# Kernel tuning notes

Measured on AMD Instinct MI355X. Metric: run time of the kernel, lower is better.

Reference implementation:

```python
import jax, jax.numpy as jnp
import numpy as np
import math

B, N, H, C = 1, 2048, 8, 128
PQ, PV, R, CS, CZ = 8, 12, 2, 256, 128
CZ4 = CZ // 4
INF = 1e5
EPS = 1e-8
SOFTPLUS_INV_1 = 0.541324854612918


def _quat_to_rot(q):
    q = q / jnp.linalg.norm(q, axis=-1, keepdims=True)
    w, x, y, z = q[..., 0], q[..., 1], q[..., 2], q[..., 3]
    return jnp.stack([
        jnp.stack([1 - 2 * (y * y + z * z), 2 * (x * y - z * w), 2 * (x * z + y * w)], -1),
        jnp.stack([2 * (x * y + z * w), 1 - 2 * (x * x + z * z), 2 * (y * z - x * w)], -1),
        jnp.stack([2 * (x * z - y * w), 2 * (y * z + x * w), 1 - 2 * (x * x + y * y)], -1),
    ], -2)


def setup_inputs() -> dict:
    key = jax.random.key(0)
    ks = jax.random.split(key, 16)
    rn = lambda k, shape, s=1.0: jax.random.normal(k, shape, dtype=jnp.float32) * s
    hc = H * C
    return dict(
        s=rn(ks[0], (B, N, CS)),
        z_factor_1=rn(ks[1], (B, N, R, CZ)),
        z_factor_2=rn(ks[2], (B, N, R, CZ)),
        rot=_quat_to_rot(rn(ks[3], (B, N, 4))),
        trans=rn(ks[4], (B, N, 3)),
        mask=jnp.ones((B, N), dtype=bool),
        w_q=rn(ks[5], (hc, CS), 0.02), b_q=jnp.zeros((hc,), jnp.float32),
        w_kv=rn(ks[6], (2 * hc, CS), 0.02), b_kv=jnp.zeros((2 * hc,), jnp.float32),
        w_qp=rn(ks[7], (H * PQ * 3, CS), 0.02), b_qp=jnp.zeros((H * PQ * 3,), jnp.float32),
        w_kvp=rn(ks[8], (H * (PQ + PV) * 3, CS), 0.02), b_kvp=jnp.zeros((H * (PQ + PV) * 3,), jnp.float32),
        w_b=rn(ks[9], (H, CZ), 0.02), b_b=jnp.zeros((H,), jnp.float32),
        w_dz=rn(ks[10], (CZ4, CZ), 0.02), b_dz=jnp.zeros((CZ4,), jnp.float32),
        head_weights=jnp.full((H,), SOFTPLUS_INV_1, dtype=jnp.float32),
        w_out=rn(ks[11], (CS, H * (CZ4 + C + 4 * PV)), 0.02), b_out=jnp.zeros((CS,), jnp.float32),
    )


def _lin(x, w, b):
    return x @ w.T + b


def _ipa(s, z1, z2, rot, trans, mask, w_q, b_q, w_kv, b_kv, w_qp, b_qp,
         w_kvp, b_kvp, w_b, b_b, w_dz, b_dz, head_weights, w_out, b_out):
    q = _lin(s, w_q, b_q).reshape(B, N, H, C)
    kv = _lin(s, w_kv, b_kv).reshape(B, N, H, 2 * C)
    k, v = kv[..., :C], kv[..., C:]
    # local points -> global frame: x_glob = R x_loc + t
    qp = _lin(s, w_qp, b_qp).reshape(B, N, H * PQ, 3)
    qp = (jnp.einsum('bnij,bnpj->bnpi', rot, qp) + trans[:, :, None, :]).reshape(B, N, H, PQ, 3)
    kvp = _lin(s, w_kvp, b_kvp).reshape(B, N, H * (PQ + PV), 3)
    kvp = (jnp.einsum('bnij,bnpj->bnpi', rot, kvp) + trans[:, :, None, :]).reshape(B, N, H, PQ + PV, 3)
    kp, vp = kvp[..., :PQ, :], kvp[..., PQ:, :]
    # head weights: softplus init to 1, AF2 scaling sqrt(1/(3*(PQ*9/2)))
    hw = jax.nn.softplus(head_weights) * math.sqrt(1.0 / (3 * (PQ * 9.0 / 2)))
    # low-rank pair bias factors
    b1 = _lin(z1, w_b, b_b)   # [B,N,R,H]
    b2 = _lin(z2, w_b, b_b)
    z1d = _lin(z1, w_dz, b_dz)  # [B,N,R,CZ4]
    z2d = _lin(z2, w_dz, b_dz)
    # logits: scalar QK + point-distance + low-rank pair bias
    scalar = jnp.einsum('bihc,bjhc->bhij', q, k) * math.sqrt(1.0 / (3 * C))
    ptdot = jnp.einsum('bihpx,bjhpx->bhij', qp, kp)
    qn = jnp.sum(qp * qp, axis=(-1, -2))  # [B,N,H]
    kn = jnp.sum(kp * kp, axis=(-1, -2))
    pt_term = hw[None, :, None, None] * (
        ptdot - 0.5 * qn.transpose(0, 2, 1)[:, :, :, None] - 0.5 * kn.transpose(0, 2, 1)[:, :, None, :])
    pair = jnp.einsum('birh,bjrh->bhij', b1, b2)
    mask_bias = jnp.where(mask, 0.0, -INF)[:, None, None, :]
    a = jax.nn.softmax(scalar + pt_term + pair + mask_bias, axis=-1)  # [B,H,N,N]
    # outputs
    o = jnp.einsum('bhij,bjhc->bihc', a, v).reshape(B, N, H * C)
    opt = jnp.einsum('bhij,bjhpx->bihpx', a, vp)  # global-frame points
    opt_loc = jnp.einsum('bnji,bnhpj->bnhpi', rot, opt - trans[:, :, None, None, :])  # R^T (x - t)
    opt_norm = jnp.sqrt(jnp.sum(opt_loc * opt_loc, axis=-1) + EPS)  # [B,N,H,PV]
    oz = jnp.einsum('bhij,bjrc->bihrc', a, z2d)
    opair = jnp.sum(oz * z1d[:, :, None, :, :], axis=3)  # [B,N,H,CZ4]
    feats = jnp.concatenate([
        o,
        opt_loc[..., 0].reshape(B, N, H * PV),
        opt_loc[..., 1].reshape(B, N, H * PV),
        opt_loc[..., 2].reshape(B, N, H * PV),
        opt_norm.reshape(B, N, H * PV),
        opair.reshape(B, N, H * CZ4),
    ], axis=-1)
    return _lin(feats, w_out, b_out)  # [B,N,CS]


def reference(s, z_factor_1, z_factor_2, rot, trans, mask, w_q, b_q, w_kv, b_kv,
              w_qp, b_qp, w_kvp, b_kvp, w_b, b_b, w_dz, b_dz, head_weights,
              w_out, b_out):
    return _ipa(s, z_factor_1, z_factor_2, rot, trans, mask, w_q, b_q, w_kv, b_kv,
                w_qp, b_qp, w_kvp, b_kvp, w_b, b_b, w_dz, b_dz, head_weights,
                w_out, b_out)
```

## Files before the change

### kernel.cpp

```cpp
#include <hip/hip_runtime.h>
#include <math.h>

#define NN   2048
#define HH   8
#define CC   128
#define PQn  8
#define PVn  12
#define RRn  2
#define CSn  256
#define CZn  128
#define CZ4n 32
#define HC   (HH*CC)
#define FEAT (HC + 4*HH*PVn + HH*CZ4n)
#define DA   160
#define DVP  256
#define DVU  240
#define QKV  3840
#define LOG2E 1.4426950408889634f

typedef unsigned short ushort_t;
#define AS1 __attribute__((address_space(1)))
#define AS3 __attribute__((address_space(3)))

using bfrag = __attribute__((ext_vector_type(8))) short;
using ffrag = __attribute__((ext_vector_type(4))) float;

__device__ inline ushort_t f2bf(float x) {
    union { float f; unsigned int u; } v; v.f = x;
    unsigned int r = v.u + 0x7fffu + ((v.u >> 16) & 1u);
    return (ushort_t)(r >> 16);
}
__device__ inline float bf2f(ushort_t x) {
    union { unsigned int u; float f; } v; v.u = ((unsigned int)x) << 16; return v.f;
}

struct CvtArgs {
    const float4* src[12];
    ushort4* dst[12];
    int n4[12];
};
__global__ __launch_bounds__(256) void cvtn_kernel(CvtArgs a,
    float4* __restrict__ outp, const float4* __restrict__ bias4)
{
    int i = blockIdx.x * 256 + threadIdx.x;
    if (i < NN * CSn / 4) {
        outp[i] = bias4[i & 63];
        return;
    }
    i -= NN * CSn / 4;
#pragma unroll
    for (int k = 0; k < 12; ++k) {
        if (i < a.n4[k]) {
            ushort4 o;
            if (a.src[k]) {
                float4 v = a.src[k][i];
                o = make_ushort4(f2bf(v.x), f2bf(v.y), f2bf(v.z), f2bf(v.w));
            } else {
                o = make_ushort4(0, 0, 0, 0);
            }
            a.dst[k][i] = o;
            return;
        }
        i -= a.n4[k];
    }
}

__global__ __launch_bounds__(256) void bgemm_kernel(
    const ushort_t* __restrict__ A, size_t sA,
    const ushort_t* __restrict__ B, size_t sB,
    void* __restrict__ Cv, size_t sC,
    const float* __restrict__ bias, size_t sBias,
    int ldk, int kOff, int kOffPerZ, int kLen, int ldc, int obf, int atomicOut)
{
    const int z = blockIdx.z;
    A += (size_t)z * sA;
    B += (size_t)z * sB;
    const float* bp = bias ? (bias + (size_t)z * sBias) : nullptr;
    const int k0beg = kOff + z * kOffPerZ;
    const int r0 = blockIdx.y * 128;
    const int c0 = blockIdx.x * 128;
    __shared__ __align__(16) ushort_t lA[128 * 32];
    __shared__ __align__(16) ushort_t lB[128 * 32];
    const int tid = threadIdx.x;
    const int w = tid >> 6, lane = tid & 63;
    const int wm = (w >> 1) * 64, wn = (w & 1) * 64;
    const int lrA = lane >> 2;
    const int lcA = (lane & 3) * 8;
    ffrag acc[4][4] = {};

    for (int k0 = k0beg; k0 < k0beg + kLen; k0 += 32) {
#pragma unroll
        for (int t = 0; t < 2; ++t) {
            int instr = w * 2 + t;
            int r = instr * 16 + lrA;
            const ushort_t* ga = A + (size_t)(r0 + r) * ldk + k0 + lcA;
            const ushort_t* gb = B + (size_t)(c0 + r) * ldk + k0 + lcA;
            __builtin_amdgcn_global_load_lds((const AS1 void*)ga,
                (AS3 void*)((AS3 ushort_t*)&lA[instr * 512 + lane * 8]), 16, 0, 0);
            __builtin_amdgcn_global_load_lds((const AS1 void*)gb,
                (AS3 void*)((AS3 ushort_t*)&lB[instr * 512 + lane * 8]), 16, 0, 0);
        }
        __syncthreads();
        bfrag af[4], bf[4];
#pragma unroll
        for (int mi = 0; mi < 4; ++mi)
            af[mi] = *(const bfrag*)&lA[(wm + mi * 16 + (lane & 15)) * 32 + (lane >> 4) * 8];
#pragma unroll
        for (int ni = 0; ni < 4; ++ni)
            bf[ni] = *(const bfrag*)&lB[(wn + ni * 16 + (lane & 15)) * 32 + (lane >> 4) * 8];
#pragma unroll
        for (int mi = 0; mi < 4; ++mi)
#pragma unroll
            for (int ni = 0; ni < 4; ++ni)
                acc[mi][ni] = __builtin_amdgcn_mfma_f32_16x16x32_bf16(af[mi], bf[ni], acc[mi][ni], 0, 0, 0);
        __syncthreads();
    }
#pragma unroll
    for (int mi = 0; mi < 4; ++mi) {
#pragma unroll
        for (int ni = 0; ni < 4; ++ni) {
            int col = c0 + wn + ni * 16 + (lane & 15);
            float bv = bp ? bp[col] : 0.f;
#pragma unroll
            for (int rr = 0; rr < 4; ++rr) {
                int row = r0 + wm + mi * 16 + (lane >> 4) * 4 + rr;
                float val = acc[mi][ni][rr] + bv;
                if (atomicOut)
                    unsafeAtomicAdd(&((float*)Cv)[(size_t)z * sC + (size_t)row * ldc + col], val);
                else if (obf)
                    ((ushort_t*)Cv)[(size_t)z * sC + (size_t)row * ldc + col] = f2bf(val);
                else
                    ((float*)Cv)[(size_t)z * sC + (size_t)row * ldc + col] = val;
            }
        }
    }
}

__global__ __launch_bounds__(256) void mgemm_kernel(
    const ushort_t* __restrict__ A0, const ushort_t* __restrict__ B0,
    ushort_t* __restrict__ C0,
    const ushort_t* __restrict__ A1, const ushort_t* __restrict__ B1,
    ushort_t* __restrict__ C1)
{
    const int bx = blockIdx.x;
    const ushort_t *A, *B;
    ushort_t* C;
    int ldk, kLen, ldc, r0, c0;
    if (bx < 480) {
        A = A0; B = B0; C = C0;
        ldk = CSn; kLen = CSn; ldc = QKV;
        r0 = (bx / 30) * 128;
        c0 = (bx % 30) * 128;
    } else {
        int i = bx - 480;
        A = A1; B = B1; C = C1;
        ldk = CZn; kLen = CZn; ldc = 128;
        r0 = i * 128;
        c0 = 0;
    }
    __shared__ __align__(16) ushort_t lA[128 * 32];
    __shared__ __align__(16) ushort_t lB[128 * 32];
    const int tid = threadIdx.x;
    const int w = tid >> 6, lane = tid & 63;
    const int wm = (w >> 1) * 64, wn = (w & 1) * 64;
    const int lrA = lane >> 2;
    const int lcA = (lane & 3) * 8;
    ffrag acc[4][4] = {};

    for (int k0 = 0; k0 < kLen; k0 += 32) {
#pragma unroll
        for (int t = 0; t < 2; ++t) {
            int instr = w * 2 + t;
            int r = instr * 16 + lrA;
            const ushort_t* ga = A + (size_t)(r0 + r) * ldk + k0 + lcA;
            const ushort_t* gb = B + (size_t)(c0 + r) * ldk + k0 + lcA;
            __builtin_amdgcn_global_load_lds((const AS1 void*)ga,
                (AS3 void*)((AS3 ushort_t*)&lA[instr * 512 + lane * 8]), 16, 0, 0);
            __builtin_amdgcn_global_load_lds((const AS1 void*)gb,
                (AS3 void*)((AS3 ushort_t*)&lB[instr * 512 + lane * 8]), 16, 0, 0);
        }
        __syncthreads();
        bfrag af[4], bf[4];
#pragma unroll
        for (int mi = 0; mi < 4; ++mi)
            af[mi] = *(const bfrag*)&lA[(wm + mi * 16 + (lane & 15)) * 32 + (lane >> 4) * 8];
#pragma unroll
        for (int ni = 0; ni < 4; ++ni)
            bf[ni] = *(const bfrag*)&lB[(wn + ni * 16 + (lane & 15)) * 32 + (lane >> 4) * 8];
#pragma unroll
        for (int mi = 0; mi < 4; ++mi)
#pragma unroll
            for (int ni = 0; ni < 4; ++ni)
                acc[mi][ni] = __builtin_amdgcn_mfma_f32_16x16x32_bf16(af[mi], bf[ni], acc[mi][ni], 0, 0, 0);
        __syncthreads();
    }
#pragma unroll
    for (int mi = 0; mi < 4; ++mi) {
#pragma unroll
        for (int ni = 0; ni < 4; ++ni) {
            int col = c0 + wn + ni * 16 + (lane & 15);
#pragma unroll
            for (int rr = 0; rr < 4; ++rr) {
                int row = r0 + wm + mi * 16 + (lane >> 4) * 4 + rr;
                C[(size_t)row * ldc + col] = f2bf(acc[mi][ni][rr]);
            }
        }
    }
}

__global__ __launch_bounds__(256) void prep_kernel(
    const ushort_t* __restrict__ qkv,
    const ushort_t* __restrict__ zproj,
    const float* __restrict__ b_q, const float* __restrict__ b_kv,
    const float* __restrict__ b_qp, const float* __restrict__ b_kvp,
    const float* __restrict__ b_b, const float* __restrict__ b_dz,
    const float* __restrict__ rot, const float* __restrict__ trans,
    const float* __restrict__ hwts,
    ushort_t* __restrict__ qaug, ushort_t* __restrict__ kaug,
    ushort_t* __restrict__ vaug)
{
    const int i = blockIdx.x;
    const int tid = threadIdx.x;
    __shared__ float R[9], t[3];
    __shared__ float qp_l[192], kp_l[192], vp_l[288];
    __shared__ float kn_s[8], hw_s[8];
    __shared__ __align__(16) ushort_t qa_s[8 * DA];
    __shared__ __align__(16) ushort_t ka_s[8 * DA];
    __shared__ __align__(16) ushort_t va_s[8 * DVP];
    if (tid < 9) R[tid] = rot[i*9 + tid];
    if (tid < 3) t[tid] = trans[i*3 + tid];
    if (tid < 8) {
        hw_s[tid] = log1pf(expf(hwts[tid])) * 0.09622504486493763f;
        kn_s[tid] = 0.f;
    }
    __syncthreads();
    if (tid < 64) {
        const ushort_t* v = qkv + (size_t)i*QKV + 3072 + tid*3;
        float vx = bf2f(v[0]) + b_qp[tid*3+0];
        float vy = bf2f(v[1]) + b_qp[tid*3+1];
        float vz = bf2f(v[2]) + b_qp[tid*3+2];
        float X = R[0]*vx + R[1]*vy + R[2]*vz + t[0];
        float Y = R[3]*vx + R[4]*vy + R[5]*vz + t[1];
        float Z = R[6]*vx + R[7]*vy + R[8]*vz + t[2];
        qp_l[tid*3+0] = X; qp_l[tid*3+1] = Y; qp_l[tid*3+2] = Z;
    } else if (tid < 224) {
        int p = tid - 64;
        int h = p / 20, pp = p % 20;
        const ushort_t* v = qkv + (size_t)i*QKV + 3264 + p*3;
        float vx = bf2f(v[0]) + b_kvp[p*3+0];
        float vy = bf2f(v[1]) + b_kvp[p*3+1];
        float vz = bf2f(v[2]) + b_kvp[p*3+2];
        float X = R[0]*vx + R[1]*vy + R[2]*vz + t[0];
        float Y = R[3]*vx + R[4]*vy + R[5]*vz + t[1];
        float Z = R[6]*vx + R[7]*vy + R[8]*vz + t[2];
        if (pp < 8) {
            int b = (h*8 + pp) * 3;
            kp_l[b+0] = X; kp_l[b+1] = Y; kp_l[b+2] = Z;
            atomicAdd(&kn_s[h], X*X + Y*Y + Z*Z);
        } else {
            int b = (h*12 + pp - 8) * 3;
            vp_l[b+0] = X; vp_l[b+1] = Y; vp_l[b+2] = Z;
        }
    }
    __syncthreads();

    const float QS = 0.05103103630798288f * LOG2E;
    if (tid < 128) {
        int h = tid >> 4, d = (tid & 15) * 8;
        bfrag q8 = *(const bfrag*)(qkv + (size_t)i*QKV + h*128 + d);
        bfrag k8 = *(const bfrag*)(qkv + (size_t)i*QKV + 1024 + h*256 + d);
        ushort_t qo[8], ko[8];
#pragma unroll
        for (int e = 0; e < 8; ++e) {
            qo[e] = f2bf(QS * (bf2f((ushort_t)q8[e]) + b_q[h*128 + d + e]));
            ko[e] = f2bf(bf2f((ushort_t)k8[e]) + b_kv[h*256 + d + e]);
        }
        *(bfrag*)&qa_s[h*DA + d] = *(bfrag*)qo;
        *(bfrag*)&ka_s[h*DA + d] = *(bfrag*)ko;
    }
    {
        int h = tid >> 5, d = 128 + (tid & 31);
        float qv, kv2;
        if (d < 152) {
            qv  = hw_s[h] * LOG2E * qp_l[h*24 + d - 128];
            kv2 = kp_l[h*24 + d - 128];
        } else if (d < 154) {
            int r = d - 152;
            qv  = LOG2E * (bf2f(zproj[(size_t)(i*2 + r)*128 + h]) + b_b[h]);
            kv2 = bf2f(zproj[(size_t)(4096 + i*2 + r)*128 + h]) + b_b[h];
        } else if (d == 154) {
            qv  = LOG2E;
            kv2 = -0.5f * hw_s[h] * kn_s[h];
        } else { qv = 0.f; kv2 = 0.f; }
        qa_s[h*DA + d] = f2bf(qv);
        ka_s[h*DA + d] = f2bf(kv2);
    }
    if (tid < 128) {
        int h = tid >> 4, d = (tid & 15) * 8;
        bfrag v8 = *(const bfrag*)(qkv + (size_t)i*QKV + 1024 + h*256 + 128 + d);
        ushort_t vo[8];
#pragma unroll
        for (int e = 0; e < 8; ++e)
            vo[e] = f2bf(bf2f((ushort_t)v8[e]) + b_kv[h*256 + 128 + d + e]);
        *(bfrag*)&va_s[h*DVP + d] = *(bfrag*)vo;
    }
#pragma unroll
    for (int k = 0; k < 4; ++k) {
        int idx = k * 256 + tid;
        int h = idx >> 7, d = 128 + (idx & 127);
        float v;
        if (d < 164)       v = vp_l[h*36 + d - 128];
        else if (d < 196)  v = bf2f(zproj[(size_t)(4096 + i*2 + 0)*128 + 8 + d - 164]) + b_dz[d - 164];
        else if (d < 228)  v = bf2f(zproj[(size_t)(4096 + i*2 + 1)*128 + 8 + d - 196]) + b_dz[d - 196];
        else if (d == 239) v = 1.0f;
        else               v = 0.f;
        va_s[h*DVP + d] = f2bf(v);
    }
    __syncthreads();

    for (int idx = tid; idx < 576; idx += 256) {
        if (idx < 160) {
            int h = idx / 20, dg = (idx - h*20) * 8;
            *(bfrag*)(qaug + ((size_t)h*NN + i) * DA + dg) = *(const bfrag*)&qa_s[h*DA + dg];
        } else if (idx < 320) {
            int r = idx - 160;
            int h = r / 20, dg = (r - h*20) * 8;
            *(bfrag*)(kaug + ((size_t)h*NN + i) * DA + dg) = *(const bfrag*)&ka_s[h*DA + dg];
        } else {
            int r = idx - 320;
            int h = r >> 5, dg = (r & 31) * 8;
            *(bfrag*)(vaug + ((size_t)h*NN + i) * DVP + dg) = *(const bfrag*)&va_s[h*DVP + dg];
        }
    }
}

__global__ __launch_bounds__(256) void transpose_kernel(
    const ushort_t* __restrict__ in, ushort_t* __restrict__ out)
{
    const int z = blockIdx.z;
    in  += (size_t)z * NN * DVP;
    out += (size_t)z * NN * DVP;
    const int i0 = blockIdx.x * 64;
    const int d0 = blockIdx.y * 64;
    __shared__ __align__(8) ushort_t tb[64][72];
    const int tid = threadIdx.x;
#pragma unroll
    for (int p = 0; p < 4; ++p) {
        int idx = p * 256 + tid;
        int r = idx >> 4, sg = idx & 15;
        ushort4 v = *(const ushort4*)(in + (size_t)(i0 + r) * DVP + d0 + sg * 4);
        *(ushort4*)&tb[r][sg * 4] = v;
    }
    __syncthreads();
#pragma unroll
    for (int p = 0; p < 4; ++p) {
        int idx = p * 256 + tid;
        int d = idx >> 4, ig = idx & 15;
        ushort4 v = make_ushort4(tb[ig*4+0][d], tb[ig*4+1][d],
                                 tb[ig*4+2][d], tb[ig*4+3][d]);
        *(ushort4*)(out + (size_t)(d0 + d) * NN + i0 + ig * 4) = v;
    }
}

__global__ __launch_bounds__(1024, 4) void flash_kernel(
    const ushort_t* __restrict__ qaug,
    const ushort_t* __restrict__ kaug,
    const ushort_t* __restrict__ vaugT,
    ushort_t* __restrict__ Opart,
    float* __restrict__ Lpart)
{
    const int bid = blockIdx.x;
    const int G = bid & 15;
    const int m = bid >> 4;
    const int h = G >> 1;
    const int g = G & 1;
    const int i0 = m * 128;

    __shared__ __align__(16) ushort_t Kt[2][64 * 168];
    __shared__ __align__(16) ushort_t Vt[2][DVU * 72];
    __shared__ __align__(16) ushort_t Pl[2][128 * 72];

    const int tid = threadIdx.x;
    const int w = tid >> 6, lane = tid & 63;
    const int quad = lane >> 4, lc = lane & 15;
    const int rq = w >> 1, jq = w & 1;
    const int rh = w >> 2, dh = (w >> 1) & 1, jc = w & 1;

    const ushort_t* qh = qaug + (size_t)h * NN * DA;
    const ushort_t* kh = kaug + (size_t)h * NN * DA;
    const ushort_t* vh = vaugT + (size_t)h * DVP * NN;

    const int j0g = g * 1024;
    const int iK0 = tid, iK1 = 1024 + tid;
    const int rK0 = iK0 / 21, oK0 = iK0 - rK0 * 21;
    const int rK1 = iK1 / 21, oK1 = iK1 - rK1 * 21;
    const bool vK1 = (tid < 320);
    const ushort_t* kS0 = kh + (size_t)(j0g + rK0) * DA + (oK0 < 20 ? oK0 * 8 : 0);
    const ushort_t* kS1 = kh + (size_t)(j0g + rK1) * DA + (oK1 < 20 ? oK1 * 8 : 0);
    const int iV0 = tid, iV1 = 1024 + tid, iV2 = 2048 + tid;
    const int rV0 = iV0 / 9, oV0 = iV0 - rV0 * 9;
    const int rV1 = iV1 / 9, oV1 = iV1 - rV1 * 9;
    const int rV2 = iV2 / 9, oV2 = iV2 - rV2 * 9;
    const bool vV2 = (tid < 112);
    const ushort_t* vS0 = vh + (size_t)rV0 * NN + j0g + (oV0 < 8 ? oV0 * 8 : 0);
    const ushort_t* vS1 = vh + (size_t)rV1 * NN + j0g + (oV1 < 8 ? oV1 * 8 : 0);
    const ushort_t* vS2 = vh + (size_t)(vV2 ? rV2 : 0) * NN + j0g + (oV2 < 8 ? oV2 * 8 : 0);

    auto stageK = [&](ushort_t* dst) {
        __builtin_amdgcn_global_load_lds((const AS1 void*)kS0,
            (AS3 void*)((AS3 ushort_t*)&dst[iK0 * 8]), 16, 0, 0);
        if (vK1)
            __builtin_amdgcn_global_load_lds((const AS1 void*)kS1,
                (AS3 void*)((AS3 ushort_t*)&dst[iK1 * 8]), 16, 0, 0);
        kS0 += 64 * DA; kS1 += 64 * DA;
    };
    auto stageV = [&](ushort_t* dst) {
        __builtin_amdgcn_global_load_lds((const AS1 void*)vS0,
            (AS3 void*)((AS3 ushort_t*)&dst[iV0 * 8]), 16, 0, 0);
        __builtin_amdgcn_global_load_lds((const AS1 void*)vS1,
            (AS3 void*)((AS3 ushort_t*)&dst[iV1 * 8]), 16, 0, 0);
        if (vV2)
            __builtin_amdgcn_global_load_lds((const AS1 void*)vS2,
                (AS3 void*)((AS3 ushort_t*)&dst[iV2 * 8]), 16, 0, 0);
        vS0 += 64; vS1 += 64; vS2 += 64;
    };

    bfrag qf[5];
#pragma unroll
    for (int ks = 0; ks < 5; ++ks)
        qf[ks] = *(const bfrag*)(qh + (size_t)(i0 + rq * 16 + lc) * DA + ks * 32 + quad * 8);

    ffrag acc[2][8];
#pragma unroll
    for (int mi = 0; mi < 2; ++mi)
#pragma unroll
        for (int t = 0; t < 8; ++t)
            acc[mi][t] = (ffrag){0.f, 0.f, 0.f, 0.f};

    stageK(Kt[0]);
    stageV(Vt[0]);
    __syncthreads();

    for (int it = 0; it < 16; ++it) {
        const int cur = it & 1;

        if (it < 15) stageK(Kt[cur ^ 1]);

        ffrag sf[2];
        sf[0] = (ffrag){0.f, 0.f, 0.f, 0.f};
        sf[1] = (ffrag){0.f, 0.f, 0.f, 0.f};
        const ushort_t* ktb = &Kt[cur][(jq * 32 + lc) * 168 + quad * 8];
        __builtin_amdgcn_s_setprio(1);
#pragma unroll
        for (int ks = 0; ks < 5; ++ks) {
            bfrag kf0 = *(const bfrag*)(ktb + ks * 32);
            bfrag kf1 = *(const bfrag*)(ktb + 16 * 168 + ks * 32);
            sf[0] = __builtin_amdgcn_mfma_f32_16x16x32_bf16(qf[ks], kf0, sf[0], 0, 0, 0);
            sf[1] = __builtin_amdgcn_mfma_f32_16x16x32_bf16(qf[ks], kf1, sf[1], 0, 0, 0);
        }

        if (it > 0) {
            const ushort_t* Plp = Pl[cur ^ 1];
            bfrag pf0 = *(const bfrag*)&Plp[(rh * 32 + lc) * 72 + jc * 32 + quad * 8];
            bfrag pf1 = *(const bfrag*)&Plp[(rh * 32 + 16 + lc) * 72 + jc * 32 + quad * 8];
            const ushort_t* vtb = &Vt[cur ^ 1][(dh * 128 + lc) * 72 + jc * 32 + quad * 8];
#pragma unroll
            for (int t = 0; t < 8; ++t) {
                if (dh && t == 7) continue;
                bfrag vf = *(const bfrag*)(vtb + t * 16 * 72);
                acc[0][t] = __builtin_amdgcn_mfma_f32_16x16x32_bf16(pf0, vf, acc[0][t], 0, 0, 0);
                acc[1][t] = __builtin_amdgcn_mfma_f32_16x16x32_bf16(pf1, vf, acc[1][t], 0, 0, 0);
            }
        }
        __builtin_amdgcn_s_setprio(0);

        {
            ushort_t* Plc = Pl[cur];
#pragma unroll
            for (int jt = 0; jt < 2; ++jt)
#pragma unroll
                for (int rr = 0; rr < 4; ++rr)
                    Plc[(rq * 16 + quad * 4 + rr) * 72 + jq * 32 + jt * 16 + lc] =
                        f2bf(exp2f(sf[jt][rr]));
        }

        __syncthreads();

        if (it < 15) stageV(Vt[cur ^ 1]);
    }

    {
        const ushort_t* Plp = Pl[1];
        bfrag pf0 = *(const bfrag*)&Plp[(rh * 32 + lc) * 72 + jc * 32 + quad * 8];
        bfrag pf1 = *(const bfrag*)&Plp[(rh * 32 + 16 + lc) * 72 + jc * 32 + quad * 8];
        const ushort_t* vtb = &Vt[1][(dh * 128 + lc) * 72 + jc * 32 + quad * 8];
#pragma unroll
        for (int t = 0; t < 8; ++t) {
            if (dh && t == 7) continue;
            bfrag vf = *(const bfrag*)(vtb + t * 16 * 72);
            acc[0][t] = __builtin_amdgcn_mfma_f32_16x16x32_bf16(pf0, vf, acc[0][t], 0, 0, 0);
            acc[1][t] = __builtin_amdgcn_mfma_f32_16x16x32_bf16(pf1, vf, acc[1][t], 0, 0, 0);
        }
    }

    ushort_t* scratch = (ushort_t*)Vt;
    const int pw = w >> 1;
    __syncthreads();
    if (jc == 1) {
        ushort_t tmp[64];
#pragma unroll
        for (int mi = 0; mi < 2; ++mi)
#pragma unroll
            for (int t = 0; t < 8; ++t)
#pragma unroll
                for (int rr = 0; rr < 4; ++rr)
                    tmp[mi*32 + t*4 + rr] = f2bf(acc[mi][t][rr]);
#pragma unroll
        for (int j = 0; j < 8; ++j)
            *(bfrag*)&scratch[pw * 4096 + j * 512 + lane * 8] = *(bfrag*)&tmp[j * 8];
    }
    __syncthreads();
    if (jc == 0) {
#pragma unroll
        for (int j = 0; j < 8; ++j) {
            bfrag v = *(const bfrag*)&scratch[pw * 4096 + j * 512 + lane * 8];
#pragma unroll
            for (int e = 0; e < 8; ++e) {
                int idx = j * 8 + e;
                acc[idx >> 5][(idx >> 2) & 7][idx & 3] += bf2f((ushort_t)v[e]);
            }
        }
        ushort_t* Ob = Opart + ((size_t)g * HH + h) * NN * DVU;
#pragma unroll
        for (int mi = 0; mi < 2; ++mi)
#pragma unroll
            for (int t = 0; t < 8; ++t) {
                if (dh && t == 7) continue;
                int dt = dh * 8 + t;
#pragma unroll
                for (int rr = 0; rr < 4; ++rr) {
                    int row = i0 + rh * 32 + mi * 16 + quad * 4 + rr;
                    Ob[(size_t)row * DVU + dt * 16 + lc] = f2bf(acc[mi][t][rr]);
                }
            }
        size_t sb = ((size_t)g * HH + h) * NN;
        if (dh == 1 && lc == 15) {
#pragma unroll
            for (int mi = 0; mi < 2; ++mi)
#pragma unroll
                for (int rr = 0; rr < 4; ++rr)
                    Lpart[sb + i0 + rh * 32 + mi * 16 + quad * 4 + rr] = acc[mi][6][rr];
        }
    }
}

__global__ __launch_bounds__(256) void combine_kernel(
    const ushort_t* __restrict__ Opart, const float* __restrict__ Lpart,
    const ushort_t* __restrict__ zproj, const float* __restrict__ b_dz,
    const float* __restrict__ rot, const float* __restrict__ trans,
    ushort_t* __restrict__ feats)
{
    const int i = blockIdx.x;
    const int tid = threadIdx.x;
    __shared__ float wgt8[8];
    __shared__ float Ol[8][DVU];
    if (tid < 8) {
        float l0 = Lpart[(size_t)(0 * HH + tid) * NN + i];
        float l1 = Lpart[(size_t)(1 * HH + tid) * NN + i];
        wgt8[tid] = 1.f / (l0 + l1);
    }
    __syncthreads();
    {
        int h = tid >> 5;
        int dg0 = tid & 31;
        for (int dg = dg0; dg < 60; dg += 32) {
            int d = dg * 4;
            ushort4 u0 = *(const ushort4*)&Opart[(((size_t)0 * HH + h) * NN + i) * DVU + d];
            ushort4 u1 = *(const ushort4*)&Opart[(((size_t)1 * HH + h) * NN + i) * DVU + d];
            float wv = wgt8[h];
            Ol[h][d+0] = (bf2f(u0.x) + bf2f(u1.x)) * wv;
            Ol[h][d+1] = (bf2f(u0.y) + bf2f(u1.y)) * wv;
            Ol[h][d+2] = (bf2f(u0.z) + bf2f(u1.z)) * wv;
            Ol[h][d+3] = (bf2f(u0.w) + bf2f(u1.w)) * wv;
        }
    }
    __syncthreads();

    ushort_t* f = feats + (size_t)i * FEAT;
    {
        int h = tid >> 5;
        int c = (tid * 4) & 127;
        ushort4 o4 = make_ushort4(f2bf(Ol[h][c]), f2bf(Ol[h][c+1]),
                                  f2bf(Ol[h][c+2]), f2bf(Ol[h][c+3]));
        *(ushort4*)(f + tid * 4) = o4;
    }
    if (tid < 96) {
        int h = tid / 12, p = tid % 12;
        const float* Rm = rot + i * 9;
        float ox = Ol[h][128 + p*3 + 0] - trans[i*3 + 0];
        float oy = Ol[h][128 + p*3 + 1] - trans[i*3 + 1];
        float oz = Ol[h][128 + p*3 + 2] - trans[i*3 + 2];
        float lx = Rm[0]*ox + Rm[3]*oy + Rm[6]*oz;
        float ly = Rm[1]*ox + Rm[4]*oy + Rm[7]*oz;
        float lz = Rm[2]*ox + Rm[5]*oy + Rm[8]*oz;
        float nrm = sqrtf(lx*lx + ly*ly + lz*lz + 1e-8f);
        f[1024 + 0*96 + tid] = f2bf(lx);
        f[1024 + 1*96 + tid] = f2bf(ly);
        f[1024 + 2*96 + tid] = f2bf(lz);
        f[1024 + 3*96 + tid] = f2bf(nrm);
    }
    {
        int h = tid >> 5, c = tid & 31;
        float z1d0 = bf2f(zproj[(size_t)(i*2 + 0)*128 + 8 + c]) + b_dz[c];
        float z1d1 = bf2f(zproj[(size_t)(i*2 + 1)*128 + 8 + c]) + b_dz[c];
        f[1408 + tid] = f2bf(Ol[h][164 + c] * z1d0 + Ol[h][196 + c] * z1d1);
    }
}

extern "C" void kernel_launch(void* const* d_in, const int* in_sizes, int n_in,
                              void* d_out, int out_size, void* d_ws, size_t ws_size,
                              hipStream_t stream) {
    const float* s     = (const float*)d_in[0];
    const float* z1    = (const float*)d_in[1];
    const float* z2    = (const float*)d_in[2];
    const float* rot   = (const float*)d_in[3];
    const float* trans = (const float*)d_in[4];
    const float* w_q   = (const float*)d_in[6];
    const float* b_q   = (const float*)d_in[7];
    const float* w_kv  = (const float*)d_in[8];
    const float* b_kv  = (const float*)d_in[9];
    const float* w_qp  = (const float*)d_in[10];
    const float* b_qp  = (const float*)d_in[11];
    const float* w_kvp = (const float*)d_in[12];
    const float* b_kvp = (const float*)d_in[13];
    const float* w_b   = (const float*)d_in[14];
    const float* b_b   = (const float*)d_in[15];
    const float* w_dz  = (const float*)d_in[16];
    const float* b_dz  = (const float*)d_in[17];
    const float* hwts  = (const float*)d_in[18];
    const float* w_out = (const float*)d_in[19];
    const float* b_out = (const float*)d_in[20];
    float* out = (float*)d_out;

    char* base = (char*)d_ws;
    const size_t OPART_BYTES = (size_t)4*HH*NN*DVU*2;
    char* S = base;
    ushort_t* s_bf  = (ushort_t*)(S);
    ushort_t* z_bf  = (ushort_t*)(S + 1048576);
    ushort_t* wall  = (ushort_t*)(S + 1048576 + 2097152);
    ushort_t* wz    = (ushort_t*)(S + 1048576 + 2097152 + 1966080);
    ushort_t* qkv   = (ushort_t*)(S + 1048576 + 2097152 + 1966080 + 32768);
    ushort_t* vaug  = (ushort_t*)(S + 1048576 + 2097152 + 1966080 + 32768 + 15728640);
    ushort_t* Opart = (ushort_t*)(S);
    char* P = base + OPART_BYTES;
    size_t off = 0;
    auto alloc = [&](size_t bytes) -> void* {
        void* p = P + off;
        off += (bytes + 255) & ~(size_t)255;
        return p;
    };
    ushort_t* wout_bf = (ushort_t*)alloc((size_t)CSn*FEAT*2);
    ushort_t* zproj   = (ushort_t*)alloc((size_t)8192*128*2);
    ushort_t* qaug    = (ushort_t*)alloc((size_t)HH*NN*DA*2);
    ushort_t* kaug    = (ushort_t*)alloc((size_t)HH*NN*DA*2);
    ushort_t* vaugT   = (ushort_t*)alloc((size_t)HH*NN*DVP*2);
    float*    Mpart   = (float*)alloc((size_t)4*HH*NN*4);
    float*    Lpart   = (float*)alloc((size_t)4*HH*NN*4);
    ushort_t* feats   = (ushort_t*)alloc((size_t)NN*FEAT*2);
    (void)Mpart;

    CvtArgs ca;
    int j = 0; int tot = 0;
    auto job = [&](const float* src, ushort_t* dst, int nElem) {
        ca.src[j] = (const float4*)src; ca.dst[j] = (ushort4*)dst; ca.n4[j] = nElem/4;
        tot += nElem/4; ++j;
    };
    job(s,     s_bf,              NN*CSn);
    job(z1,    z_bf,              4096*128);
    job(z2,    z_bf + 4096*128,   4096*128);
    job(w_q,   wall,              1024*256);
    job(w_kv,  wall + 1024*256,   2048*256);
    job(w_qp,  wall + 3072*256,   192*256);
    job(w_kvp, wall + 3264*256,   480*256);
    job(w_out, wout_bf,           CSn*FEAT);
    job(nullptr, wall + 3744*256, 96*256);
    job(w_b,   wz,                8*128);
    job(w_dz,  wz + 8*128,        32*128);
    job(nullptr, wz + 40*128,     88*128);
    tot += NN*CSn/4;
    cvtn_kernel<<<(tot + 255)/256, 256, 0, stream>>>(ca, (float4*)out, (const float4*)b_out);

    mgemm_kernel<<<544, 256, 0, stream>>>(s_bf, wall, qkv, z_bf, wz, zproj);

    prep_kernel<<<NN, 256, 0, stream>>>(qkv, zproj,
                                        b_q, b_kv, b_qp, b_kvp, b_b, b_dz,
                                        rot, trans, hwts, qaug, kaug, vaug);
    transpose_kernel<<<dim3(NN/64, DVP/64, HH), 256, 0, stream>>>(vaug, vaugT);

    flash_kernel<<<256, 1024, 0, stream>>>(
        qaug, kaug, vaugT, Opart, Lpart);

    combine_kernel<<<NN, 256, 0, stream>>>(Opart, Lpart, zproj, b_dz,
                                           rot, trans, feats);

    bgemm_kernel<<<dim3(CSn/128, NN/128, 4), 256, 0, stream>>>(
        feats, 0, wout_bf, 0, out, 0, nullptr, 0,
        FEAT, 0, FEAT/4, FEAT/4, CSn, 0, 1);
}
```

Before: 194.0 us.

## Fuse all stages into one persistent megakernel with grid-wide atomic barriers

Replaces the seven separate launches (convert, projection GEMMs, prep, transpose, flash attention, combine, output GEMM) with a single persistent kernel of 256 blocks of 1024 threads. The stages are separated by a software grid barrier built on an atomic counter. Each stage's work is remapped onto four 256-thread crews per block. This removes launch overhead and the inter-kernel gaps, but depends on all 256 blocks being co-resident. It also forces every stage onto the same block shape and shared-memory budget, which may lower per-stage efficiency.

```diff
diff --git a/kernel.cpp b/kernel.cpp
--- a/kernel.cpp
+++ b/kernel.cpp
@@ -34,436 +34,400 @@
     union { unsigned int u; float f; } v; v.u = ((unsigned int)x) << 16; return v.f;
 }
 
+#define GLOAD(src, dst) __builtin_amdgcn_global_load_lds((const AS1 void*)(src), \
+    (AS3 void*)((AS3 ushort_t*)(dst)), 16, 0, 0)
+
 struct CvtArgs {
     const float4* src[12];
     ushort4* dst[12];
     int n4[12];
 };
-__global__ __launch_bounds__(256) void cvtn_kernel(CvtArgs a,
-    float4* __restrict__ outp, const float4* __restrict__ bias4)
-{
-    int i = blockIdx.x * 256 + threadIdx.x;
-    if (i < NN * CSn / 4) {
-        outp[i] = bias4[i & 63];
-        return;
-    }
-    i -= NN * CSn / 4;
-#pragma unroll
-    for (int k = 0; k < 12; ++k) {
-        if (i < a.n4[k]) {
-            ushort4 o;
-            if (a.src[k]) {
-                float4 v = a.src[k][i];
-                o = make_ushort4(f2bf(v.x), f2bf(v.y), f2bf(v.z), f2bf(v.w));
-            } else {
-                o = make_ushort4(0, 0, 0, 0);
-            }
-            a.dst[k][i] = o;
-            return;
-        }
-        i -= a.n4[k];
-    }
+
+__device__ inline void gsync(unsigned* cnt, unsigned target) {
+    __syncthreads();
+    if (threadIdx.x == 0) {
+        __threadfence();
+        atomicAdd(cnt, 1u);
+        while (atomicAdd(cnt, 0u) < target) __builtin_amdgcn_s_sleep(8);
+        __threadfence();
+    }
+    __syncthreads();
 }
 
-__global__ __launch_bounds__(256) void bgemm_kernel(
-    const ushort_t* __restrict__ A, size_t sA,
-    const ushort_t* __restrict__ B, size_t sB,
-    void* __restrict__ Cv, size_t sC,
-    const float* __restrict__ bias, size_t sBias,
-    int ldk, int kOff, int kOffPerZ, int kLen, int ldc, int obf, int atomicOut)
-{
-    const int z = blockIdx.z;
-    A += (size_t)z * sA;
-    B += (size_t)z * sB;
-    const float* bp = bias ? (bias + (size_t)z * sBias) : nullptr;
-    const int k0beg = kOff + z * kOffPerZ;
-    const int r0 = blockIdx.y * 128;
-    const int c0 = blockIdx.x * 128;
-    __shared__ __align__(16) ushort_t lA[128 * 32];
-    __shared__ __align__(16) ushort_t lB[128 * 32];
-    const int tid = threadIdx.x;
-    const int w = tid >> 6, lane = tid & 63;
-    const int wm = (w >> 1) * 64, wn = (w & 1) * 64;
-    const int lrA = lane >> 2;
-    const int lcA = (lane & 3) * 8;
-    ffrag acc[4][4] = {};
-
-    for (int k0 = k0beg; k0 < k0beg + kLen; k0 += 32) {
-#pragma unroll
-        for (int t = 0; t < 2; ++t) {
-            int instr = w * 2 + t;
-            int r = instr * 16 + lrA;
-            const ushort_t* ga = A + (size_t)(r0 + r) * ldk + k0 + lcA;
-            const ushort_t* gb = B + (size_t)(c0 + r) * ldk + k0 + lcA;
-            __builtin_amdgcn_global_load_lds((const AS1 void*)ga,
-                (AS3 void*)((AS3 ushort_t*)&lA[instr * 512 + lane * 8]), 16, 0, 0);
-            __builtin_amdgcn_global_load_lds((const AS1 void*)gb,
-                (AS3 void*)((AS3 ushort_t*)&lB[instr * 512 + lane * 8]), 16, 0, 0);
-        }
-        __syncthreads();
-        bfrag af[4], bf[4];
-#pragma unroll
-        for (int mi = 0; mi < 4; ++mi)
-            af[mi] = *(const bfrag*)&lA[(wm + mi * 16 + (lane & 15)) * 32 + (lane >> 4) * 8];
-#pragma unroll
-        for (int ni = 0; ni < 4; ++ni)
-            bf[ni] = *(const bfrag*)&lB[(wn + ni * 16 + (lane & 15)) * 32 + (lane >> 4) * 8];
-#pragma unroll
-        for (int mi = 0; mi < 4; ++mi)
-#pragma unroll
-            for (int ni = 0; ni < 4; ++ni)
-                acc[mi][ni] = __builtin_amdgcn_mfma_f32_16x16x32_bf16(af[mi], bf[ni], acc[mi][ni], 0, 0, 0);
-        __syncthreads();
-    }
-#pragma unroll
-    for (int mi = 0; mi < 4; ++mi) {
-#pragma unroll
-        for (int ni = 0; ni < 4; ++ni) {
-            int col = c0 + wn + ni * 16 + (lane & 15);
-            float bv = bp ? bp[col] : 0.f;
-#pragma unroll
-            for (int rr = 0; rr < 4; ++rr) {
-                int row = r0 + wm + mi * 16 + (lane >> 4) * 4 + rr;
-                float val = acc[mi][ni][rr] + bv;
-                if (atomicOut)
-                    unsafeAtomicAdd(&((float*)Cv)[(size_t)z * sC + (size_t)row * ldc + col], val);
-                else if (obf)
-                    ((ushort_t*)Cv)[(size_t)z * sC + (size_t)row * ldc + col] = f2bf(val);
-                else
-                    ((float*)Cv)[(size_t)z * sC + (size_t)row * ldc + col] = val;
-            }
-        }
-    }
-}
-
-__global__ __launch_bounds__(256) void mgemm_kernel(
-    const ushort_t* __restrict__ A0, const ushort_t* __restrict__ B0,
-    ushort_t* __restrict__ C0,
-    const ushort_t* __restrict__ A1, const ushort_t* __restrict__ B1,
-    ushort_t* __restrict__ C1)
-{
-    const int bx = blockIdx.x;
-    const ushort_t *A, *B;
-    ushort_t* C;
-    int ldk, kLen, ldc, r0, c0;
-    if (bx < 480) {
-        A = A0; B = B0; C = C0;
-        ldk = CSn; kLen = CSn; ldc = QKV;
-        r0 = (bx / 30) * 128;
-        c0 = (bx % 30) * 128;
-    } else {
-        int i = bx - 480;
-        A = A1; B = B1; C = C1;
-        ldk = CZn; kLen = CZn; ldc = 128;
-        r0 = i * 128;
-        c0 = 0;
-    }
-    __shared__ __align__(16) ushort_t lA[128 * 32];
-    __shared__ __align__(16) ushort_t lB[128 * 32];
-    const int tid = threadIdx.x;
-    const int w = tid >> 6, lane = tid & 63;
-    const int wm = (w >> 1) * 64, wn = (w & 1) * 64;
-    const int lrA = lane >> 2;
-    const int lcA = (lane & 3) * 8;
-    ffrag acc[4][4] = {};
-
-    for (int k0 = 0; k0 < kLen; k0 += 32) {
-#pragma unroll
-        for (int t = 0; t < 2; ++t) {
-            int instr = w * 2 + t;
-            int r = instr * 16 + lrA;
-            const ushort_t* ga = A + (size_t)(r0 + r) * ldk + k0 + lcA;
-            const ushort_t* gb = B + (size_t)(c0 + r) * ldk + k0 + lcA;
-            __builtin_amdgcn_global_load_lds((const AS1 void*)ga,
-                (AS3 void*)((AS3 ushort_t*)&lA[instr * 512 + lane * 8]), 16, 0, 0);
-            __builtin_amdgcn_global_load_lds((const AS1 void*)gb,
-                (AS3 void*)((AS3 ushort_t*)&lB[instr * 512 + lane * 8]), 16, 0, 0);
-        }
-        __syncthreads();
-        bfrag af[4], bf[4];
-#pragma unroll
-        for (int mi = 0; mi < 4; ++mi)
-            af[mi] = *(const bfrag*)&lA[(wm + mi * 16 + (lane & 15)) * 32 + (lane >> 4) * 8];
-#pragma unroll
-        for (int ni = 0; ni < 4; ++ni)
-            bf[ni] = *(const bfrag*)&lB[(wn + ni * 16 + (lane & 15)) * 32 + (lane >> 4) * 8];
-#pragma unroll
-        for (int mi = 0; mi < 4; ++mi)
-#pragma unroll
-            for (int ni = 0; ni < 4; ++ni)
-                acc[mi][ni] = __builtin_amdgcn_mfma_f32_16x16x32_bf16(af[mi], bf[ni], acc[mi][ni], 0, 0, 0);
-        __syncthreads();
-    }
-#pragma unroll
-    for (int mi = 0; mi < 4; ++mi) {
-#pragma unroll
-        for (int ni = 0; ni < 4; ++ni) {
-            int col = c0 + wn + ni * 16 + (lane & 15);
-#pragma unroll
-            for (int rr = 0; rr < 4; ++rr) {
-                int row = r0 + wm + mi * 16 + (lane >> 4) * 4 + rr;
-                C[(size_t)row * ldc + col] = f2bf(acc[mi][ni][rr]);
-            }
-        }
-    }
-}
-
-__global__ __launch_bounds__(256) void prep_kernel(
-    const ushort_t* __restrict__ qkv,
-    const ushort_t* __restrict__ zproj,
+struct PrepShm {
+    float R[9], t[3];
+    float qp_l[192], kp_l[192], vp_l[288];
+    float kn_s[8], hw_s[8];
+    __align__(16) ushort_t qa_s[8 * DA];
+    __align__(16) ushort_t ka_s[8 * DA];
+    __align__(16) ushort_t va_s[8 * DVP];
+};
+struct CombShm {
+    float wgt8[8];
+    float Ol[8][DVU];
+};
+
+__global__ __launch_bounds__(1024, 4) void mega_kernel(
+    CvtArgs ca, float4* __restrict__ outp, const float4* __restrict__ bias4, int cvtTot,
+    const ushort_t* __restrict__ s_bf, const ushort_t* __restrict__ wall,
+    ushort_t* __restrict__ qkv, const ushort_t* __restrict__ z_bf,
+    const ushort_t* __restrict__ wz, ushort_t* __restrict__ zproj,
     const float* __restrict__ b_q, const float* __restrict__ b_kv,
     const float* __restrict__ b_qp, const float* __restrict__ b_kvp,
     const float* __restrict__ b_b, const float* __restrict__ b_dz,
     const float* __restrict__ rot, const float* __restrict__ trans,
     const float* __restrict__ hwts,
     ushort_t* __restrict__ qaug, ushort_t* __restrict__ kaug,
-    ushort_t* __restrict__ vaug)
+    ushort_t* __restrict__ vaug, ushort_t* __restrict__ vaugT,
+    ushort_t* __restrict__ Opart, float* __restrict__ Lpart,
+    ushort_t* __restrict__ feats, const ushort_t* __restrict__ wout_bf,
+    float* __restrict__ out, unsigned* __restrict__ syncnt)
 {
-    const int i = blockIdx.x;
+    __shared__ __align__(16) char smem[148992];
     const int tid = threadIdx.x;
-    __shared__ float R[9], t[3];
-    __shared__ float qp_l[192], kp_l[192], vp_l[288];
-    __shared__ float kn_s[8], hw_s[8];
-    __shared__ __align__(16) ushort_t qa_s[8 * DA];
-    __shared__ __align__(16) ushort_t ka_s[8 * DA];
-    __shared__ __align__(16) ushort_t va_s[8 * DVP];
-    if (tid < 9) R[tid] = rot[i*9 + tid];
-    if (tid < 3) t[tid] = trans[i*3 + tid];
-    if (tid < 8) {
-        hw_s[tid] = log1pf(expf(hwts[tid])) * 0.09622504486493763f;
-        kn_s[tid] = 0.f;
-    }
-    __syncthreads();
-    if (tid < 64) {
-        const ushort_t* v = qkv + (size_t)i*QKV + 3072 + tid*3;
-        float vx = bf2f(v[0]) + b_qp[tid*3+0];
-        float vy = bf2f(v[1]) + b_qp[tid*3+1];
-        float vz = bf2f(v[2]) + b_qp[tid*3+2];
-        float X = R[0]*vx + R[1]*vy + R[2]*vz + t[0];
-        float Y = R[3]*vx + R[4]*vy + R[5]*vz + t[1];
-        float Z = R[6]*vx + R[7]*vy + R[8]*vz + t[2];
-        qp_l[tid*3+0] = X; qp_l[tid*3+1] = Y; qp_l[tid*3+2] = Z;
-    } else if (tid < 224) {
-        int p = tid - 64;
-        int h = p / 20, pp = p % 20;
-        const ushort_t* v = qkv + (size_t)i*QKV + 3264 + p*3;
-        float vx = bf2f(v[0]) + b_kvp[p*3+0];
-        float vy = bf2f(v[1]) + b_kvp[p*3+1];
-        float vz = bf2f(v[2]) + b_kvp[p*3+2];
-        float X = R[0]*vx + R[1]*vy + R[2]*vz + t[0];
-        float Y = R[3]*vx + R[4]*vy + R[5]*vz + t[1];
-        float Z = R[6]*vx + R[7]*vy + R[8]*vz + t[2];
-        if (pp < 8) {
-            int b = (h*8 + pp) * 3;
-            kp_l[b+0] = X; kp_l[b+1] = Y; kp_l[b+2] = Z;
-            atomicAdd(&kn_s[h], X*X + Y*Y + Z*Z);
-        } else {
-            int b = (h*12 + pp - 8) * 3;
-            vp_l[b+0] = X; vp_l[b+1] = Y; vp_l[b+2] = Z;
-        }
-    }
-    __syncthreads();
-
-    const float QS = 0.05103103630798288f * LOG2E;
-    if (tid < 128) {
-        int h = tid >> 4, d = (tid & 15) * 8;
-        bfrag q8 = *(const bfrag*)(qkv + (size_t)i*QKV + h*128 + d);
-        bfrag k8 = *(const bfrag*)(qkv + (size_t)i*QKV + 1024 + h*256 + d);
-        ushort_t qo[8], ko[8];
-#pragma unroll
-        for (int e = 0; e < 8; ++e) {
-            qo[e] = f2bf(QS * (bf2f((ushort_t)q8[e]) + b_q[h*128 + d + e]));
-            ko[e] = f2bf(bf2f((ushort_t)k8[e]) + b_kv[h*256 + d + e]);
-        }
-        *(bfrag*)&qa_s[h*DA + d] = *(bfrag*)qo;
-        *(bfrag*)&ka_s[h*DA + d] = *(bfrag*)ko;
-    }
+    const int bid = blockIdx.x;
+    const int crew = tid >> 8, ctid = tid & 255;
+
     {
-        int h = tid >> 5, d = 128 + (tid & 31);
-        float qv, kv2;
-        if (d < 152) {
-            qv  = hw_s[h] * LOG2E * qp_l[h*24 + d - 128];
-            kv2 = kp_l[h*24 + d - 128];
-        } else if (d < 154) {
-            int r = d - 152;
-            qv  = LOG2E * (bf2f(zproj[(size_t)(i*2 + r)*128 + h]) + b_b[h]);
-            kv2 = bf2f(zproj[(size_t)(4096 + i*2 + r)*128 + h]) + b_b[h];
-        } else if (d == 154) {
-            qv  = LOG2E;
-            kv2 = -0.5f * hw_s[h] * kn_s[h];
-        } else { qv = 0.f; kv2 = 0.f; }
-        qa_s[h*DA + d] = f2bf(qv);
-        ka_s[h*DA + d] = f2bf(kv2);
-    }
-    if (tid < 128) {
-        int h = tid >> 4, d = (tid & 15) * 8;
-        bfrag v8 = *(const bfrag*)(qkv + (size_t)i*QKV + 1024 + h*256 + 128 + d);
-        ushort_t vo[8];
-#pragma unroll
-        for (int e = 0; e < 8; ++e)
-            vo[e] = f2bf(bf2f((ushort_t)v8[e]) + b_kv[h*256 + 128 + d + e]);
-        *(bfrag*)&va_s[h*DVP + d] = *(bfrag*)vo;
-    }
-#pragma unroll
-    for (int k = 0; k < 4; ++k) {
-        int idx = k * 256 + tid;
-        int h = idx >> 7, d = 128 + (idx & 127);
-        float v;
-        if (d < 164)       v = vp_l[h*36 + d - 128];
-        else if (d < 196)  v = bf2f(zproj[(size_t)(4096 + i*2 + 0)*128 + 8 + d - 164]) + b_dz[d - 164];
-        else if (d < 228)  v = bf2f(zproj[(size_t)(4096 + i*2 + 1)*128 + 8 + d - 196]) + b_dz[d - 196];
-        else if (d == 239) v = 1.0f;
-        else               v = 0.f;
-        va_s[h*DVP + d] = f2bf(v);
-    }
-    __syncthreads();
-
-    for (int idx = tid; idx < 576; idx += 256) {
-        if (idx < 160) {
-            int h = idx / 20, dg = (idx - h*20) * 8;
-            *(bfrag*)(qaug + ((size_t)h*NN + i) * DA + dg) = *(const bfrag*)&qa_s[h*DA + dg];
-        } else if (idx < 320) {
-            int r = idx - 160;
-            int h = r / 20, dg = (r - h*20) * 8;
-            *(bfrag*)(kaug + ((size_t)h*NN + i) * DA + dg) = *(const bfrag*)&ka_s[h*DA + dg];
-        } else {
-            int r = idx - 320;
-            int h = r >> 5, dg = (r & 31) * 8;
-            *(bfrag*)(vaug + ((size_t)h*NN + i) * DVP + dg) = *(const bfrag*)&va_s[h*DVP + dg];
-        }
-    }
-}
-
-__global__ __launch_bounds__(256) void transpose_kernel(
-    const ushort_t* __restrict__ in, ushort_t* __restrict__ out)
-{
-    const int z = blockIdx.z;
-    in  += (size_t)z * NN * DVP;
-    out += (size_t)z * NN * DVP;
-    const int i0 = blockIdx.x * 64;
-    const int d0 = blockIdx.y * 64;
-    __shared__ __align__(8) ushort_t tb[64][72];
-    const int tid = threadIdx.x;
-#pragma unroll
-    for (int p = 0; p < 4; ++p) {
-        int idx = p * 256 + tid;
-        int r = idx >> 4, sg = idx & 15;
-        ushort4 v = *(const ushort4*)(in + (size_t)(i0 + r) * DVP + d0 + sg * 4);
-        *(ushort4*)&tb[r][sg * 4] = v;
-    }
-    __syncthreads();
-#pragma unroll
-    for (int p = 0; p < 4; ++p) {
-        int idx = p * 256 + tid;
-        int d = idx >> 4, ig = idx & 15;
-        ushort4 v = make_ushort4(tb[ig*4+0][d], tb[ig*4+1][d],
-                                 tb[ig*4+2][d], tb[ig*4+3][d]);
-        *(ushort4*)(out + (size_t)(d0 + d) * NN + i0 + ig * 4) = v;
-    }
-}
-
-__global__ __launch_bounds__(1024, 4) void flash_kernel(
-    const ushort_t* __restrict__ qaug,
-    const ushort_t* __restrict__ kaug,
-    const ushort_t* __restrict__ vaugT,
-    ushort_t* __restrict__ Opart,
-    float* __restrict__ Lpart)
-{
-    const int bid = blockIdx.x;
-    const int G = bid & 15;
-    const int m = bid >> 4;
-    const int h = G >> 1;
-    const int g = G & 1;
-    const int i0 = m * 128;
-
-    __shared__ __align__(16) ushort_t Kt[2][64 * 168];
-    __shared__ __align__(16) ushort_t Vt[2][DVU * 72];
-    __shared__ __align__(16) ushort_t Pl[2][128 * 72];
-
-    const int tid = threadIdx.x;
-    const int w = tid >> 6, lane = tid & 63;
-    const int quad = lane >> 4, lc = lane & 15;
-    const int rq = w >> 1, jq = w & 1;
-    const int rh = w >> 2, dh = (w >> 1) & 1, jc = w & 1;
-
-    const ushort_t* qh = qaug + (size_t)h * NN * DA;
-    const ushort_t* kh = kaug + (size_t)h * NN * DA;
-    const ushort_t* vh = vaugT + (size_t)h * DVP * NN;
-
-    const int j0g = g * 1024;
-    const int iK0 = tid, iK1 = 1024 + tid;
-    const int rK0 = iK0 / 21, oK0 = iK0 - rK0 * 21;
-    const int rK1 = iK1 / 21, oK1 = iK1 - rK1 * 21;
-    const bool vK1 = (tid < 320);
-    const ushort_t* kS0 = kh + (size_t)(j0g + rK0) * DA + (oK0 < 20 ? oK0 * 8 : 0);
-    const ushort_t* kS1 = kh + (size_t)(j0g + rK1) * DA + (oK1 < 20 ? oK1 * 8 : 0);
-    const int iV0 = tid, iV1 = 1024 + tid, iV2 = 2048 + tid;
-    const int rV0 = iV0 / 9, oV0 = iV0 - rV0 * 9;
-    const int rV1 = iV1 / 9, oV1 = iV1 - rV1 * 9;
-    const int rV2 = iV2 / 9, oV2 = iV2 - rV2 * 9;
-    const bool vV2 = (tid < 112);
-    const ushort_t* vS0 = vh + (size_t)rV0 * NN + j0g + (oV0 < 8 ? oV0 * 8 : 0);
-    const ushort_t* vS1 = vh + (size_t)rV1 * NN + j0g + (oV1 < 8 ? oV1 * 8 : 0);
-    const ushort_t* vS2 = vh + (size_t)(vV2 ? rV2 : 0) * NN + j0g + (oV2 < 8 ? oV2 * 8 : 0);
-
-    auto stageK = [&](ushort_t* dst) {
-        __builtin_amdgcn_global_load_lds((const AS1 void*)kS0,
-            (AS3 void*)((AS3 ushort_t*)&dst[iK0 * 8]), 16, 0, 0);
-        if (vK1)
-            __builtin_amdgcn_global_load_lds((const AS1 void*)kS1,
-                (AS3 void*)((AS3 ushort_t*)&dst[iK1 * 8]), 16, 0, 0);
-        kS0 += 64 * DA; kS1 += 64 * DA;
-    };
-    auto stageV = [&](ushort_t* dst) {
-        __builtin_amdgcn_global_load_lds((const AS1 void*)vS0,
-            (AS3 void*)((AS3 ushort_t*)&dst[iV0 * 8]), 16, 0, 0);
-        __builtin_amdgcn_global_load_lds((const AS1 void*)vS1,
-            (AS3 void*)((AS3 ushort_t*)&dst[iV1 * 8]), 16, 0, 0);
-        if (vV2)
-            __builtin_amdgcn_global_load_lds((const AS1 void*)vS2,
-                (AS3 void*)((AS3 ushort_t*)&dst[iV2 * 8]), 16, 0, 0);
-        vS0 += 64; vS1 += 64; vS2 += 64;
-    };
-
-    bfrag qf[5];
-#pragma unroll
-    for (int ks = 0; ks < 5; ++ks)
-        qf[ks] = *(const bfrag*)(qh + (size_t)(i0 + rq * 16 + lc) * DA + ks * 32 + quad * 8);
-
-    ffrag acc[2][8];
-#pragma unroll
-    for (int mi = 0; mi < 2; ++mi)
-#pragma unroll
-        for (int t = 0; t < 8; ++t)
-            acc[mi][t] = (ffrag){0.f, 0.f, 0.f, 0.f};
-
-    stageK(Kt[0]);
-    stageV(Vt[0]);
-    __syncthreads();
-
-    for (int it = 0; it < 16; ++it) {
-        const int cur = it & 1;
-
-        if (it < 15) stageK(Kt[cur ^ 1]);
-
-        ffrag sf[2];
-        sf[0] = (ffrag){0.f, 0.f, 0.f, 0.f};
-        sf[1] = (ffrag){0.f, 0.f, 0.f, 0.f};
-        const ushort_t* ktb = &Kt[cur][(jq * 32 + lc) * 168 + quad * 8];
-        __builtin_amdgcn_s_setprio(1);
-#pragma unroll
-        for (int ks = 0; ks < 5; ++ks) {
-            bfrag kf0 = *(const bfrag*)(ktb + ks * 32);
-            bfrag kf1 = *(const bfrag*)(ktb + 16 * 168 + ks * 32);
-            sf[0] = __builtin_amdgcn_mfma_f32_16x16x32_bf16(qf[ks], kf0, sf[0], 0, 0, 0);
-            sf[1] = __builtin_amdgcn_mfma_f32_16x16x32_bf16(qf[ks], kf1, sf[1], 0, 0, 0);
-        }
-
-        if (it > 0) {
-            const ushort_t* Plp = Pl[cur ^ 1];
+        const int STRIDE = 256 * 1024;
+        for (int it = bid * 1024 + tid; it < cvtTot; it += STRIDE) {
+            int r = it;
+            if (r < NN * CSn / 4) { outp[r] = bias4[r & 63]; continue; }
+            r -= NN * CSn / 4;
+#pragma unroll
+            for (int k = 0; k < 12; ++k) {
+                if (r < ca.n4[k]) {
+                    ushort4 o;
+                    if (ca.src[k]) {
+                        float4 v = ca.src[k][r];
+                        o = make_ushort4(f2bf(v.x), f2bf(v.y), f2bf(v.z), f2bf(v.w));
+                    } else {
+                        o = make_ushort4(0, 0, 0, 0);
+                    }
+                    ca.dst[k][r] = o;
+                    r = -1; break;
+                }
+                r -= ca.n4[k];
+            }
+        }
+    }
+    gsync(syncnt, 256 * 1);
+
+    {
+        const int vb = bid + 256 * crew;
+        const bool active = vb < 544;
+        const ushort_t *A = s_bf, *B = wall;
+        ushort_t* C = qkv;
+        int ldk = CSn, kIters = 8, ldc = QKV, r0 = 0, c0 = 0;
+        if (vb < 480) { r0 = (vb / 30) * 128; c0 = (vb % 30) * 128; }
+        else if (active) { int i2 = vb - 480; A = z_bf; B = wz; C = zproj;
+                           ldk = CZn; kIters = 4; ldc = 128; r0 = i2 * 128; c0 = 0; }
+        ushort_t* lA = (ushort_t*)(smem + crew * 16384);
+        ushort_t* lB = lA + 4096;
+        const int w4 = ctid >> 6, lane = ctid & 63;
+        const int wm = (w4 >> 1) * 64, wn = (w4 & 1) * 64;
+        const int lrA = lane >> 2, lcA = (lane & 3) * 8;
+        ffrag acc[4][4] = {};
+        for (int kk = 0; kk < 8; ++kk) {
+            bool act = active && (kk < kIters);
+            if (act) {
+                int k0 = kk * 32;
+#pragma unroll
+                for (int t = 0; t < 2; ++t) {
+                    int instr = w4 * 2 + t;
+                    int r = instr * 16 + lrA;
+                    GLOAD(A + (size_t)(r0 + r) * ldk + k0 + lcA, &lA[instr * 512 + lane * 8]);
+                    GLOAD(B + (size_t)(c0 + r) * ldk + k0 + lcA, &lB[instr * 512 + lane * 8]);
+                }
+            }
+            __syncthreads();
+            if (act) {
+                bfrag af[4], bf[4];
+#pragma unroll
+                for (int mi = 0; mi < 4; ++mi)
+                    af[mi] = *(const bfrag*)&lA[(wm + mi * 16 + (lane & 15)) * 32 + (lane >> 4) * 8];
+#pragma unroll
+                for (int ni = 0; ni < 4; ++ni)
+                    bf[ni] = *(const bfrag*)&lB[(wn + ni * 16 + (lane & 15)) * 32 + (lane >> 4) * 8];
+#pragma unroll
+                for (int mi = 0; mi < 4; ++mi)
+#pragma unroll
+                    for (int ni = 0; ni < 4; ++ni)
+                        acc[mi][ni] = __builtin_amdgcn_mfma_f32_16x16x32_bf16(af[mi], bf[ni], acc[mi][ni], 0, 0, 0);
+            }
+            __syncthreads();
+        }
+        if (active) {
+#pragma unroll
+            for (int mi = 0; mi < 4; ++mi)
+#pragma unroll
+                for (int ni = 0; ni < 4; ++ni) {
+                    int col = c0 + wn + ni * 16 + (lane & 15);
+#pragma unroll
+                    for (int rr = 0; rr < 4; ++rr) {
+                        int row = r0 + wm + mi * 16 + (lane >> 4) * 4 + rr;
+                        C[(size_t)row * ldc + col] = f2bf(acc[mi][ni][rr]);
+                    }
+                }
+        }
+    }
+    gsync(syncnt, 256 * 2);
+
+    {
+        PrepShm* ps = (PrepShm*)(smem + crew * 12016);
+        for (int rep = 0; rep < 2; ++rep) {
+            const int i = bid * 8 + crew * 2 + rep;
+            if (ctid < 9) ps->R[ctid] = rot[i * 9 + ctid];
+            if (ctid < 3) ps->t[ctid] = trans[i * 3 + ctid];
+            if (ctid < 8) {
+                ps->hw_s[ctid] = log1pf(expf(hwts[ctid])) * 0.09622504486493763f;
+                ps->kn_s[ctid] = 0.f;
+            }
+            __syncthreads();
+            if (ctid < 64) {
+                const ushort_t* v = qkv + (size_t)i * QKV + 3072 + ctid * 3;
+                float vx = bf2f(v[0]) + b_qp[ctid * 3 + 0];
+                float vy = bf2f(v[1]) + b_qp[ctid * 3 + 1];
+                float vz = bf2f(v[2]) + b_qp[ctid * 3 + 2];
+                float X = ps->R[0] * vx + ps->R[1] * vy + ps->R[2] * vz + ps->t[0];
+                float Y = ps->R[3] * vx + ps->R[4] * vy + ps->R[5] * vz + ps->t[1];
+                float Z = ps->R[6] * vx + ps->R[7] * vy + ps->R[8] * vz + ps->t[2];
+                ps->qp_l[ctid * 3 + 0] = X; ps->qp_l[ctid * 3 + 1] = Y; ps->qp_l[ctid * 3 + 2] = Z;
+            } else if (ctid < 224) {
+                int p = ctid - 64;
+                int h = p / 20, pp = p % 20;
+                const ushort_t* v = qkv + (size_t)i * QKV + 3264 + p * 3;
+                float vx = bf2f(v[0]) + b_kvp[p * 3 + 0];
+                float vy = bf2f(v[1]) + b_kvp[p * 3 + 1];
+                float vz = bf2f(v[2]) + b_kvp[p * 3 + 2];
+                float X = ps->R[0] * vx + ps->R[1] * vy + ps->R[2] * vz + ps->t[0];
+                float Y = ps->R[3] * vx + ps->R[4] * vy + ps->R[5] * vz + ps->t[1];
+                float Z = ps->R[6] * vx + ps->R[7] * vy + ps->R[8] * vz + ps->t[2];
+                if (pp < 8) {
+                    int b = (h * 8 + pp) * 3;
+                    ps->kp_l[b + 0] = X; ps->kp_l[b + 1] = Y; ps->kp_l[b + 2] = Z;
+                    atomicAdd(&ps->kn_s[h], X * X + Y * Y + Z * Z);
+                } else {
+                    int b = (h * 12 + pp - 8) * 3;
+                    ps->vp_l[b + 0] = X; ps->vp_l[b + 1] = Y; ps->vp_l[b + 2] = Z;
+                }
+            }
+            __syncthreads();
+
+            const float QS = 0.05103103630798288f * LOG2E;
+            if (ctid < 128) {
+                int h = ctid >> 4, d = (ctid & 15) * 8;
+                bfrag q8 = *(const bfrag*)(qkv + (size_t)i * QKV + h * 128 + d);
+                bfrag k8 = *(const bfrag*)(qkv + (size_t)i * QKV + 1024 + h * 256 + d);
+                ushort_t qo[8], ko[8];
+#pragma unroll
+                for (int e = 0; e < 8; ++e) {
+                    qo[e] = f2bf(QS * (bf2f((ushort_t)q8[e]) + b_q[h * 128 + d + e]));
+                    ko[e] = f2bf(bf2f((ushort_t)k8[e]) + b_kv[h * 256 + d + e]);
+                }
+                *(bfrag*)&ps->qa_s[h * DA + d] = *(bfrag*)qo;
+                *(bfrag*)&ps->ka_s[h * DA + d] = *(bfrag*)ko;
+            }
+            {
+                int h = ctid >> 5, d = 128 + (ctid & 31);
+                float qv, kv2;
+                if (d < 152) {
+                    qv  = ps->hw_s[h] * LOG2E * ps->qp_l[h * 24 + d - 128];
+                    kv2 = ps->kp_l[h * 24 + d - 128];
+                } else if (d < 154) {
+                    int r = d - 152;
+                    qv  = LOG2E * (bf2f(zproj[(size_t)(i * 2 + r) * 128 + h]) + b_b[h]);
+                    kv2 = bf2f(zproj[(size_t)(4096 + i * 2 + r) * 128 + h]) + b_b[h];
+                } else if (d == 154) {
+                    qv  = LOG2E;
+                    kv2 = -0.5f * ps->hw_s[h] * ps->kn_s[h];
+                } else { qv = 0.f; kv2 = 0.f; }
+                ps->qa_s[h * DA + d] = f2bf(qv);
+                ps->ka_s[h * DA + d] = f2bf(kv2);
+            }
+            if (ctid < 128) {
+                int h = ctid >> 4, d = (ctid & 15) * 8;
+                bfrag v8 = *(const bfrag*)(qkv + (size_t)i * QKV + 1024 + h * 256 + 128 + d);
+                ushort_t vo[8];
+#pragma unroll
+                for (int e = 0; e < 8; ++e)
+                    vo[e] = f2bf(bf2f((ushort_t)v8[e]) + b_kv[h * 256 + 128 + d + e]);
+                *(bfrag*)&ps->va_s[h * DVP + d] = *(bfrag*)vo;
+            }
+#pragma unroll
+            for (int k = 0; k < 4; ++k) {
+                int idx = k * 256 + ctid;
+                int h = idx >> 7, d = 128 + (idx & 127);
+                float v;
+                if (d < 164)       v = ps->vp_l[h * 36 + d - 128];
+                else if (d < 196)  v = bf2f(zproj[(size_t)(4096 + i * 2 + 0) * 128 + 8 + d - 164]) + b_dz[d - 164];
+                else if (d < 228)  v = bf2f(zproj[(size_t)(4096 + i * 2 + 1) * 128 + 8 + d - 196]) + b_dz[d - 196];
+                else if (d == 239) v = 1.0f;
+                else               v = 0.f;
+                ps->va_s[h * DVP + d] = f2bf(v);
+            }
+            __syncthreads();
+
+            for (int idx = ctid; idx < 576; idx += 256) {
+                if (idx < 160) {
+                    int h = idx / 20, dg = (idx - h * 20) * 8;
+                    *(bfrag*)(qaug + ((size_t)h * NN + i) * DA + dg) = *(const bfrag*)&ps->qa_s[h * DA + dg];
+                } else if (idx < 320) {
+                    int r = idx - 160;
+                    int h = r / 20, dg = (r - h * 20) * 8;
+                    *(bfrag*)(kaug + ((size_t)h * NN + i) * DA + dg) = *(const bfrag*)&ps->ka_s[h * DA + dg];
+                } else {
+                    int r = idx - 320;
+                    int h = r >> 5, dg = (r & 31) * 8;
+                    *(bfrag*)(vaug + ((size_t)h * NN + i) * DVP + dg) = *(const bfrag*)&ps->va_s[h * DVP + dg];
+                }
+            }
+            __syncthreads();
+        }
+    }
+    gsync(syncnt, 256 * 3);
+
+    {
+        const int vb = bid + 256 * crew;
+        const int x = vb & 31, y = (vb >> 5) & 3, z = vb >> 7;
+        const ushort_t* in  = vaug  + (size_t)z * NN * DVP;
+        ushort_t*       outT = vaugT + (size_t)z * NN * DVP;
+        const int i0 = x * 64, d0 = y * 64;
+        ushort_t* tb = (ushort_t*)(smem + crew * 9216);
+#pragma unroll
+        for (int p = 0; p < 4; ++p) {
+            int idx = p * 256 + ctid;
+            int r = idx >> 4, sg = idx & 15;
+            ushort4 v = *(const ushort4*)(in + (size_t)(i0 + r) * DVP + d0 + sg * 4);
+            *(ushort4*)&tb[r * 72 + sg * 4] = v;
+        }
+        __syncthreads();
+#pragma unroll
+        for (int p = 0; p < 4; ++p) {
+            int idx = p * 256 + ctid;
+            int d = idx >> 4, ig = idx & 15;
+            ushort4 v = make_ushort4(tb[(ig * 4 + 0) * 72 + d], tb[(ig * 4 + 1) * 72 + d],
+                                     tb[(ig * 4 + 2) * 72 + d], tb[(ig * 4 + 3) * 72 + d]);
+            *(ushort4*)(outT + (size_t)(d0 + d) * NN + i0 + ig * 4) = v;
+        }
+    }
+    gsync(syncnt, 256 * 4);
+
+    {
+        ushort_t* const KtB = (ushort_t*)smem;
+        ushort_t* const VtB = (ushort_t*)smem + 21504;
+        ushort_t* const PlB = (ushort_t*)smem + 56064;
+#define KT(b)  (KtB + (b) * 10752)
+#define VT(b)  (VtB + (b) * 17280)
+#define PLBUF(b) (PlB + (b) * 9216)
+
+        const int G = bid & 15;
+        const int m = bid >> 4;
+        const int h = G >> 1;
+        const int g = G & 1;
+        const int i0 = m * 128;
+
+        const int w = tid >> 6, lane = tid & 63;
+        const int quad = lane >> 4, lc = lane & 15;
+        const int rq = w >> 1, jq = w & 1;
+        const int rh = w >> 2, dh = (w >> 1) & 1, jc = w & 1;
+
+        const ushort_t* qh = qaug + (size_t)h * NN * DA;
+        const ushort_t* kh = kaug + (size_t)h * NN * DA;
+        const ushort_t* vh = vaugT + (size_t)h * DVP * NN;
+
+        const int j0g = g * 1024;
+        const int iK0 = tid, iK1 = 1024 + tid;
+        const int rK0 = iK0 / 21, oK0 = iK0 - rK0 * 21;
+        const int rK1 = iK1 / 21, oK1 = iK1 - rK1 * 21;
+        const bool vK1 = (tid < 320);
+        const ushort_t* kS0 = kh + (size_t)(j0g + rK0) * DA + (oK0 < 20 ? oK0 * 8 : 0);
+        const ushort_t* kS1 = kh + (size_t)(j0g + rK1) * DA + (oK1 < 20 ? oK1 * 8 : 0);
+        const int iV0 = tid, iV1 = 1024 + tid, iV2 = 2048 + tid;
+        const int rV0 = iV0 / 9, oV0 = iV0 - rV0 * 9;
+        const int rV1 = iV1 / 9, oV1 = iV1 - rV1 * 9;
+        const int rV2 = iV2 / 9, oV2 = iV2 - rV2 * 9;
+        const bool vV2 = (tid < 112);
+        const ushort_t* vS0 = vh + (size_t)rV0 * NN + j0g + (oV0 < 8 ? oV0 * 8 : 0);
+        const ushort_t* vS1 = vh + (size_t)rV1 * NN + j0g + (oV1 < 8 ? oV1 * 8 : 0);
+        const ushort_t* vS2 = vh + (size_t)(vV2 ? rV2 : 0) * NN + j0g + (oV2 < 8 ? oV2 * 8 : 0);
+
+        auto stageK = [&](ushort_t* dst) {
+            GLOAD(kS0, &dst[iK0 * 8]);
+            if (vK1) GLOAD(kS1, &dst[iK1 * 8]);
+            kS0 += 64 * DA; kS1 += 64 * DA;
+        };
+        auto stageV = [&](ushort_t* dst) {
+            GLOAD(vS0, &dst[iV0 * 8]);
+            GLOAD(vS1, &dst[iV1 * 8]);
+            if (vV2) GLOAD(vS2, &dst[iV2 * 8]);
+            vS0 += 64; vS1 += 64; vS2 += 64;
+        };
+
+        bfrag qf[5];
+#pragma unroll
+        for (int ks = 0; ks < 5; ++ks)
+            qf[ks] = *(const bfrag*)(qh + (size_t)(i0 + rq * 16 + lc) * DA + ks * 32 + quad * 8);
+
+        ffrag acc[2][8];
+#pragma unroll
+        for (int mi = 0; mi < 2; ++mi)
+#pragma unroll
+            for (int t = 0; t < 8; ++t)
+                acc[mi][t] = (ffrag){0.f, 0.f, 0.f, 0.f};
+
+        stageK(KT(0));
+        stageV(VT(0));
+        __syncthreads();
+
+        for (int it = 0; it < 16; ++it) {
+            const int cur = it & 1;
+            if (it < 15) stageK(KT(cur ^ 1));
+
+            ffrag sf[2];
+            sf[0] = (ffrag){0.f, 0.f, 0.f, 0.f};
+            sf[1] = (ffrag){0.f, 0.f, 0.f, 0.f};
+            const ushort_t* ktb = KT(cur) + (jq * 32 + lc) * 168 + quad * 8;
+            __builtin_amdgcn_s_setprio(1);
+#pragma unroll
+            for (int ks = 0; ks < 5; ++ks) {
+                bfrag kf0 = *(const bfrag*)(ktb + ks * 32);
+                bfrag kf1 = *(const bfrag*)(ktb + 16 * 168 + ks * 32);
+                sf[0] = __builtin_amdgcn_mfma_f32_16x16x32_bf16(qf[ks], kf0, sf[0], 0, 0, 0);
+                sf[1] = __builtin_amdgcn_mfma_f32_16x16x32_bf16(qf[ks], kf1, sf[1], 0, 0, 0);
+            }
+            if (it > 0) {
+                const ushort_t* Plp = PLBUF(cur ^ 1);
+                bfrag pf0 = *(const bfrag*)&Plp[(rh * 32 + lc) * 72 + jc * 32 + quad * 8];
+                bfrag pf1 = *(const bfrag*)&Plp[(rh * 32 + 16 + lc) * 72 + jc * 32 + quad * 8];
+                const ushort_t* vtb = VT(cur ^ 1) + (dh * 128 + lc) * 72 + jc * 32 + quad * 8;
+#pragma unroll
+                for (int t = 0; t < 8; ++t) {
+                    if (dh && t == 7) continue;
+                    bfrag vf = *(const bfrag*)(vtb + t * 16 * 72);
+                    acc[0][t] = __builtin_amdgcn_mfma_f32_16x16x32_bf16(pf0, vf, acc[0][t], 0, 0, 0);
+                    acc[1][t] = __builtin_amdgcn_mfma_f32_16x16x32_bf16(pf1, vf, acc[1][t], 0, 0, 0);
+                }
+            }
+            __builtin_amdgcn_s_setprio(0);
+            {
+                ushort_t* Plc = PLBUF(cur);
+#pragma unroll
+                for (int jt = 0; jt < 2; ++jt)
+#pragma unroll
+                    for (int rr = 0; rr < 4; ++rr)
+                        Plc[(rq * 16 + quad * 4 + rr) * 72 + jq * 32 + jt * 16 + lc] =
+                            f2bf(exp2f(sf[jt][rr]));
+            }
+            __syncthreads();
+            if (it < 15) stageV(VT(cur ^ 1));
+        }
+
+        {
+            const ushort_t* Plp = PLBUF(1);
             bfrag pf0 = *(const bfrag*)&Plp[(rh * 32 + lc) * 72 + jc * 32 + quad * 8];
             bfrag pf1 = *(const bfrag*)&Plp[(rh * 32 + 16 + lc) * 72 + jc * 32 + quad * 8];
-            const ushort_t* vtb = &Vt[cur ^ 1][(dh * 128 + lc) * 72 + jc * 32 + quad * 8];
+            const ushort_t* vtb = VT(1) + (dh * 128 + lc) * 72 + jc * 32 + quad * 8;
 #pragma unroll
             for (int t = 0; t < 8; ++t) {
                 if (dh && t == 7) continue;
@@ -472,148 +436,177 @@
                 acc[1][t] = __builtin_amdgcn_mfma_f32_16x16x32_bf16(pf1, vf, acc[1][t], 0, 0, 0);
             }
         }
-        __builtin_amdgcn_s_setprio(0);
-
-        {
-            ushort_t* Plc = Pl[cur];
-#pragma unroll
-            for (int jt = 0; jt < 2; ++jt)
-#pragma unroll
-                for (int rr = 0; rr < 4; ++rr)
-                    Plc[(rq * 16 + quad * 4 + rr) * 72 + jq * 32 + jt * 16 + lc] =
-                        f2bf(exp2f(sf[jt][rr]));
-        }
-
+
+        ushort_t* scratch = VT(0);
+        const int pw = w >> 1;
         __syncthreads();
-
-        if (it < 15) stageV(Vt[cur ^ 1]);
-    }
+        if (jc == 1) {
+            ushort_t tmp[64];
+#pragma unroll
+            for (int mi = 0; mi < 2; ++mi)
+#pragma unroll
+                for (int t = 0; t < 8; ++t)
+#pragma unroll
+                    for (int rr = 0; rr < 4; ++rr)
+                        tmp[mi * 32 + t * 4 + rr] = f2bf(acc[mi][t][rr]);
+#pragma unroll
+            for (int j = 0; j < 8; ++j)
+                *(bfrag*)&scratch[pw * 4096 + j * 512 + lane * 8] = *(bfrag*)&tmp[j * 8];
+        }
+        __syncthreads();
+        if (jc == 0) {
+#pragma unroll
+            for (int j = 0; j < 8; ++j) {
+                bfrag v = *(const bfrag*)&scratch[pw * 4096 + j * 512 + lane * 8];
+#pragma unroll
+                for (int e = 0; e < 8; ++e) {
+                    int idx = j * 8 + e;
+                    acc[idx >> 5][(idx >> 2) & 7][idx & 3] += bf2f((ushort_t)v[e]);
+                }
+            }
+            ushort_t* Ob = Opart + ((size_t)g * HH + h) * NN * DVU;
+#pragma unroll
+            for (int mi = 0; mi < 2; ++mi)
+#pragma unroll
+                for (int t = 0; t < 8; ++t) {
+                    if (dh && t == 7) continue;
+                    int dt = dh * 8 + t;
+#pragma unroll
+                    for (int rr = 0; rr < 4; ++rr) {
+                        int row = i0 + rh * 32 + mi * 16 + quad * 4 + rr;
+                        Ob[(size_t)row * DVU + dt * 16 + lc] = f2bf(acc[mi][t][rr]);
+                    }
+                }
+            size_t sb = ((size_t)g * HH + h) * NN;
+            if (dh == 1 && lc == 15) {
+#pragma unroll
+                for (int mi = 0; mi < 2; ++mi)
+#pragma unroll
+                    for (int rr = 0; rr < 4; ++rr)
+                        Lpart[sb + i0 + rh * 32 + mi * 16 + quad * 4 + rr] = acc[mi][6][rr];
+            }
+        }
+#undef KT
+#undef VT
+#undef PLBUF
+    }
+    gsync(syncnt, 256 * 5);
 
     {
-        const ushort_t* Plp = Pl[1];
-        bfrag pf0 = *(const bfrag*)&Plp[(rh * 32 + lc) * 72 + jc * 32 + quad * 8];
-        bfrag pf1 = *(const bfrag*)&Plp[(rh * 32 + 16 + lc) * 72 + jc * 32 + quad * 8];
-        const ushort_t* vtb = &Vt[1][(dh * 128 + lc) * 72 + jc * 32 + quad * 8];
-#pragma unroll
-        for (int t = 0; t < 8; ++t) {
-            if (dh && t == 7) continue;
-            bfrag vf = *(const bfrag*)(vtb + t * 16 * 72);
-            acc[0][t] = __builtin_amdgcn_mfma_f32_16x16x32_bf16(pf0, vf, acc[0][t], 0, 0, 0);
-            acc[1][t] = __builtin_amdgcn_mfma_f32_16x16x32_bf16(pf1, vf, acc[1][t], 0, 0, 0);
-        }
-    }
-
-    ushort_t* scratch = (ushort_t*)Vt;
-    const int pw = w >> 1;
-    __syncthreads();
-    if (jc == 1) {
-        ushort_t tmp[64];
-#pragma unroll
-        for (int mi = 0; mi < 2; ++mi)
-#pragma unroll
-            for (int t = 0; t < 8; ++t)
-#pragma unroll
-                for (int rr = 0; rr < 4; ++rr)
-                    tmp[mi*32 + t*4 + rr] = f2bf(acc[mi][t][rr]);
-#pragma unroll
-        for (int j = 0; j < 8; ++j)
-            *(bfrag*)&scratch[pw * 4096 + j * 512 + lane * 8] = *(bfrag*)&tmp[j * 8];
-    }
-    __syncthreads();
-    if (jc == 0) {
-#pragma unroll
-        for (int j = 0; j < 8; ++j) {
-            bfrag v = *(const bfrag*)&scratch[pw * 4096 + j * 512 + lane * 8];
-#pragma unroll
-            for (int e = 0; e < 8; ++e) {
-                int idx = j * 8 + e;
-                acc[idx >> 5][(idx >> 2) & 7][idx & 3] += bf2f((ushort_t)v[e]);
-            }
-        }
-        ushort_t* Ob = Opart + ((size_t)g * HH + h) * NN * DVU;
-#pragma unroll
-        for (int mi = 0; mi < 2; ++mi)
-#pragma unroll
-            for (int t = 0; t < 8; ++t) {
-                if (dh && t == 7) continue;
-                int dt = dh * 8 + t;
-#pragma unroll
-                for (int rr = 0; rr < 4; ++rr) {
-                    int row = i0 + rh * 32 + mi * 16 + quad * 4 + rr;
-                    Ob[(size_t)row * DVU + dt * 16 + lc] = f2bf(acc[mi][t][rr]);
-                }
-            }
-        size_t sb = ((size_t)g * HH + h) * NN;
-        if (dh == 1 && lc == 15) {
-#pragma unroll
-            for (int mi = 0; mi < 2; ++mi)
-#pragma unroll
-                for (int rr = 0; rr < 4; ++rr)
-                    Lpart[sb + i0 + rh * 32 + mi * 16 + quad * 4 + rr] = acc[mi][6][rr];
-        }
-    }
-}
-
-__global__ __launch_bounds__(256) void combine_kernel(
-    const ushort_t* __restrict__ Opart, const float* __restrict__ Lpart,
-    const ushort_t* __restrict__ zproj, const float* __restrict__ b_dz,
-    const float* __restrict__ rot, const float* __restrict__ trans,
-    ushort_t* __restrict__ feats)
-{
-    const int i = blockIdx.x;
-    const int tid = threadIdx.x;
-    __shared__ float wgt8[8];
-    __shared__ float Ol[8][DVU];
-    if (tid < 8) {
-        float l0 = Lpart[(size_t)(0 * HH + tid) * NN + i];
-        float l1 = Lpart[(size_t)(1 * HH + tid) * NN + i];
-        wgt8[tid] = 1.f / (l0 + l1);
-    }
-    __syncthreads();
+        CombShm* cs = (CombShm*)(smem + crew * 7712);
+        for (int rep = 0; rep < 2; ++rep) {
+            const int i = bid * 8 + crew * 2 + rep;
+            if (ctid < 8) {
+                float l0 = Lpart[(size_t)(0 * HH + ctid) * NN + i];
+                float l1 = Lpart[(size_t)(1 * HH + ctid) * NN + i];
+                cs->wgt8[ctid] = 1.f / (l0 + l1);
+            }
+            __syncthreads();
+            {
+                int h = ctid >> 5;
+                int dg0 = ctid & 31;
+                for (int dg = dg0; dg < 60; dg += 32) {
+                    int d = dg * 4;
+                    ushort4 u0 = *(const ushort4*)&Opart[(((size_t)0 * HH + h) * NN + i) * DVU + d];
+                    ushort4 u1 = *(const ushort4*)&Opart[(((size_t)1 * HH + h) * NN + i) * DVU + d];
+                    float wv = cs->wgt8[h];
+                    cs->Ol[h][d + 0] = (bf2f(u0.x) + bf2f(u1.x)) * wv;
+                    cs->Ol[h][d + 1] = (bf2f(u0.y) + bf2f(u1.y)) * wv;
+                    cs->Ol[h][d + 2] = (bf2f(u0.z) + bf2f(u1.z)) * wv;
+                    cs->Ol[h][d + 3] = (bf2f(u0.w) + bf2f(u1.w)) * wv;
+                }
+            }
+            __syncthreads();
+
+            ushort_t* f = feats + (size_t)i * FEAT;
+            {
+                int h = ctid >> 5;
+                int c = (ctid * 4) & 127;
+                ushort4 o4 = make_ushort4(f2bf(cs->Ol[h][c]), f2bf(cs->Ol[h][c + 1]),
+                                          f2bf(cs->Ol[h][c + 2]), f2bf(cs->Ol[h][c + 3]));
+                *(ushort4*)(f + ctid * 4) = o4;
+            }
+            if (ctid < 96) {
+                int h = ctid / 12, p = ctid % 12;
+                const float* Rm = rot + i * 9;
+                float ox = cs->Ol[h][128 + p * 3 + 0] - trans[i * 3 + 0];
+                float oy = cs->Ol[h][128 + p * 3 + 1] - trans[i * 3 + 1];
+                float oz = cs->Ol[h][128 + p * 3 + 2] - trans[i * 3 + 2];
+                float lx = Rm[0] * ox + Rm[3] * oy + Rm[6] * oz;
+                float ly = Rm[1] * ox + Rm[4] * oy + Rm[7] * oz;
+                float lz = Rm[2] * ox + Rm[5] * oy + Rm[8] * oz;
+                float nrm = sqrtf(lx * lx + ly * ly + lz * lz + 1e-8f);
+                f[1024 + 0 * 96 + ctid] = f2bf(lx);
+                f[1024 + 1 * 96 + ctid] = f2bf(ly);
+                f[1024 + 2 * 96 + ctid] = f2bf(lz);
+                f[1024 + 3 * 96 + ctid] = f2bf(nrm);
+            }
+            {
+                int h = ctid >> 5, c = ctid & 31;
+                float z1d0 = bf2f(zproj[(size_t)(i * 2 + 0) * 128 + 8 + c]) + b_dz[c];
+                float z1d1 = bf2f(zproj[(size_t)(i * 2 + 1) * 128 + 8 + c]) + b_dz[c];
+                f[1408 + ctid] = f2bf(cs->Ol[h][164 + c] * z1d0 + cs->Ol[h][196 + c] * z1d1);
+            }
+            __syncthreads();
+        }
+    }
+    gsync(syncnt, 256 * 6);
+
     {
-        int h = tid >> 5;
-        int dg0 = tid & 31;
-        for (int dg = dg0; dg < 60; dg += 32) {
-            int d = dg * 4;
-            ushort4 u0 = *(const ushort4*)&Opart[(((size_t)0 * HH + h) * NN + i) * DVU + d];
-            ushort4 u1 = *(const ushort4*)&Opart[(((size_t)1 * HH + h) * NN + i) * DVU + d];
-            float wv = wgt8[h];
-            Ol[h][d+0] = (bf2f(u0.x) + bf2f(u1.x)) * wv;
-            Ol[h][d+1] = (bf2f(u0.y) + bf2f(u1.y)) * wv;
-            Ol[h][d+2] = (bf2f(u0.z) + bf2f(u1.z)) * wv;
-            Ol[h][d+3] = (bf2f(u0.w) + bf2f(u1.w)) * wv;
-        }
-    }
-    __syncthreads();
-
-    ushort_t* f = feats + (size_t)i * FEAT;
-    {
-        int h = tid >> 5;
-        int c = (tid * 4) & 127;
-        ushort4 o4 = make_ushort4(f2bf(Ol[h][c]), f2bf(Ol[h][c+1]),
-                                  f2bf(Ol[h][c+2]), f2bf(Ol[h][c+3]));
-        *(ushort4*)(f + tid * 4) = o4;
-    }
-    if (tid < 96) {
-        int h = tid / 12, p = tid % 12;
-        const float* Rm = rot + i * 9;
-        float ox = Ol[h][128 + p*3 + 0] - trans[i*3 + 0];
-        float oy = Ol[h][128 + p*3 + 1] - trans[i*3 + 1];
-        float oz = Ol[h][128 + p*3 + 2] - trans[i*3 + 2];
-        float lx = Rm[0]*ox + Rm[3]*oy + Rm[6]*oz;
-        float ly = Rm[1]*ox + Rm[4]*oy + Rm[7]*oz;
-        float lz = Rm[2]*ox + Rm[5]*oy + Rm[8]*oz;
-        float nrm = sqrtf(lx*lx + ly*ly + lz*lz + 1e-8f);
-        f[1024 + 0*96 + tid] = f2bf(lx);
-        f[1024 + 1*96 + tid] = f2bf(ly);
-        f[1024 + 2*96 + tid] = f2bf(lz);
-        f[1024 + 3*96 + tid] = f2bf(nrm);
-    }
-    {
-        int h = tid >> 5, c = tid & 31;
-        float z1d0 = bf2f(zproj[(size_t)(i*2 + 0)*128 + 8 + c]) + b_dz[c];
-        float z1d1 = bf2f(zproj[(size_t)(i*2 + 1)*128 + 8 + c]) + b_dz[c];
-        f[1408 + tid] = f2bf(Ol[h][164 + c] * z1d0 + Ol[h][196 + c] * z1d1);
+        const int vb = bid + 256 * crew;
+        const bool active = vb < 416;
+        const int z = active ? (vb / 32) : 0;
+        const int rem = active ? (vb % 32) : 0;
+        const int c0 = (rem & 1) * 128;
+        const int r0 = (rem >> 1) * 128;
+        const int kbeg = z * 128;
+        ushort_t* lA = (ushort_t*)(smem + crew * 16384);
+        ushort_t* lB = lA + 4096;
+        const int w4 = ctid >> 6, lane = ctid & 63;
+        const int wm = (w4 >> 1) * 64, wn = (w4 & 1) * 64;
+        const int lrA = lane >> 2, lcA = (lane & 3) * 8;
+        ffrag acc[4][4] = {};
+        for (int kk = 0; kk < 4; ++kk) {
+            if (active) {
+                int k0 = kbeg + kk * 32;
+#pragma unroll
+                for (int t = 0; t < 2; ++t) {
+                    int instr = w4 * 2 + t;
+                    int r = instr * 16 + lrA;
+                    GLOAD(feats   + (size_t)(r0 + r) * FEAT + k0 + lcA, &lA[instr * 512 + lane * 8]);
+                    GLOAD(wout_bf + (size_t)(c0 + r) * FEAT + k0 + lcA, &lB[instr * 512 + lane * 8]);
+                }
+            }
+            __syncthreads();
+            if (active) {
+                bfrag af[4], bf[4];
+#pragma unroll
+                for (int mi = 0; mi < 4; ++mi)
+                    af[mi] = *(const bfrag*)&lA[(wm + mi * 16 + (lane & 15)) * 32 + (lane >> 4) * 8];
+#pragma unroll
+                for (int ni = 0; ni < 4; ++ni)
+                    bf[ni] = *(const bfrag*)&lB[(wn + ni * 16 + (lane & 15)) * 32 + (lane >> 4) * 8];
+#pragma unroll
+                for (int mi = 0; mi < 4; ++mi)
+#pragma unroll
+                    for (int ni = 0; ni < 4; ++ni)
+                        acc[mi][ni] = __builtin_amdgcn_mfma_f32_16x16x32_bf16(af[mi], bf[ni], acc[mi][ni], 0, 0, 0);
+            }
+            __syncthreads();
+        }
+        if (active) {
+#pragma unroll
+            for (int mi = 0; mi < 4; ++mi)
+#pragma unroll
+                for (int ni = 0; ni < 4; ++ni) {
+                    int col = c0 + wn + ni * 16 + (lane & 15);
+#pragma unroll
+                    for (int rr = 0; rr < 4; ++rr) {
+                        int row = r0 + wm + mi * 16 + (lane >> 4) * 4 + rr;
+                        unsafeAtomicAdd(&out[(size_t)row * CSn + col], acc[mi][ni][rr]);
+                    }
+                }
+        }
     }
 }
 
@@ -667,6 +660,7 @@
     float*    Mpart   = (float*)alloc((size_t)4*HH*NN*4);
     float*    Lpart   = (float*)alloc((size_t)4*HH*NN*4);
     ushort_t* feats   = (ushort_t*)alloc((size_t)NN*FEAT*2);
+    unsigned* syncnt  = (unsigned*)alloc(256);
     (void)Mpart;
 
     CvtArgs ca;
@@ -688,22 +682,12 @@
     job(w_dz,  wz + 8*128,        32*128);
     job(nullptr, wz + 40*128,     88*128);
     tot += NN*CSn/4;
-    cvtn_kernel<<<(tot + 255)/256, 256, 0, stream>>>(ca, (float4*)out, (const float4*)b_out);
-
-    mgemm_kernel<<<544, 256, 0, stream>>>(s_bf, wall, qkv, z_bf, wz, zproj);
-
-    prep_kernel<<<NN, 256, 0, stream>>>(qkv, zproj,
-                                        b_q, b_kv, b_qp, b_kvp, b_b, b_dz,
-                                        rot, trans, hwts, qaug, kaug, vaug);
-    transpose_kernel<<<dim3(NN/64, DVP/64, HH), 256, 0, stream>>>(vaug, vaugT);
-
-    flash_kernel<<<256, 1024, 0, stream>>>(
-        qaug, kaug, vaugT, Opart, Lpart);
-
-    combine_kernel<<<NN, 256, 0, stream>>>(Opart, Lpart, zproj, b_dz,
-                                           rot, trans, feats);
-
-    bgemm_kernel<<<dim3(CSn/128, NN/128, 4), 256, 0, stream>>>(
-        feats, 0, wout_bf, 0, out, 0, nullptr, 0,
-        FEAT, 0, FEAT/4, FEAT/4, CSn, 0, 1);
+
+    hipMemsetAsync(syncnt, 0, sizeof(unsigned), stream);
+    mega_kernel<<<256, 1024, 0, stream>>>(
+        ca, (float4*)out, (const float4*)b_out, tot,
+        s_bf, wall, qkv, z_bf, wz, zproj,
+        b_q, b_kv, b_qp, b_kvp, b_b, b_dz, rot, trans, hwts,
+        qaug, kaug, vaug, vaugT,
+        Opart, Lpart, feats, wout_bf, out, syncnt);
 }
```

Result: slower. 359.0 us (+85.1%).
